# Performance work log

Hardware: AMD Instinct MI355X
Metric: run time of the kernel (lower is better)

## Reference

```python
import jax, jax.numpy as jnp
import numpy as np

B, T, N, F = 8, 24, 207, 16
H = 64            # hidden_dim
DH = 16           # dims_hyper[-1] / node-embedding out
DA = 4 * F        # temporal attention dim_out
DS = 64           # ss_gal gcn out dim (last_ss_gal_dim)
GDEP = 2
ALPHA, BETA, GAMMA = 0.05, 0.95, 0.95
TA = 2.0


def _lin(x, w, b=None):
    y = x @ w
    return y if b is None else y + b


def gcn_hyper(x, A, W, b):
    # x: [B,N,C], A: [N,N] static. h <- a*x + g * einsum('nvc,vw->nwc', h, A)
    h = x
    outs = [h]
    for _ in range(GDEP):
        h = ALPHA * x + GAMMA * jnp.einsum('bvc,vw->bwc', h, A)
        outs.append(h)
    return _lin(jnp.concatenate(outs, axis=-1), W, b)


def gcn_gru(x, A_dyn, A_sta, W, b):
    # x: [B,N,C], A_dyn: [B,N,N], A_sta: [N,N]
    h = x
    outs = [h]
    for _ in range(GDEP):
        h = (ALPHA * x
             + BETA * jnp.einsum('bvw,bvc->bwc', A_dyn, h)     # bmm(A^T, h)
             + GAMMA * jnp.einsum('bvc,vw->bwc', h, A_sta))
        outs.append(h)
    return _lin(jnp.concatenate(outs, axis=-1), W, b)


def gcn_ssgal(x, A, W, b):
    # x: [B*,N,C], A: [B*,N,N]
    h = x
    outs = [h]
    for _ in range(GDEP):
        h = ALPHA * x + GAMMA * jnp.einsum('bvw,bvc->bwc', A, h)
        outs.append(h)
    return _lin(jnp.concatenate(outs, axis=-1), W, b)


def setup_inputs() -> dict:
    key = jax.random.key(0)
    ks = jax.random.split(key, 32)
    i = iter(range(32))
    w = lambda *s: (0.02 * jax.random.normal(ks[next(i)], s, dtype=jnp.float32))
    inp = {
        'input_sequence': jax.random.normal(ks[next(i)], (B, T, N, F), dtype=jnp.float32),
        'static_adj': jax.random.uniform(ks[next(i)], (N, N), dtype=jnp.float32),
        # hyper graph generators: mlp in = (GDEP+1)*H -> DH
        'src_gen_w': w((GDEP + 1) * H, DH), 'src_gen_b': w(DH),
        'tgt_gen_w': w((GDEP + 1) * H, DH), 'tgt_gen_b': w(DH),
        # node embeddings: F -> DH
        'src_emb_w': w(F, DH), 'src_emb_b': w(DH),
        'tgt_emb_w': w(F, DH), 'tgt_emb_b': w(DH),
        # GRU gate GCNs: mlp in = (GDEP+1)*(F+H) -> H
        'gru_z_w': w((GDEP + 1) * (F + H), H), 'gru_z_b': w(H),
        'gru_r_w': w((GDEP + 1) * (F + H), H), 'gru_r_b': w(H),
        'gru_c_w': w((GDEP + 1) * (F + H), H), 'gru_c_b': w(H),
        # temporal attention: F -> DA, score DA -> 1
        'attn_q_w': w(F, DA),
        'attn_k_w': w(F, DA), 'attn_k_b': w(DA),
        'attn_s_w': w(DA, 1),
        # ss_gal spatial gcn: (GDEP+1)*F -> DS
        'sgcn_w': w((GDEP + 1) * F, DS), 'sgcn_b': w(DS),
        # predictors
        'short_w': w(DS, F), 'short_b': w(F),
        'long_w': w(H, F), 'long_b': w(F),
        'fus_w': w(DS + H, F), 'fus_b': w(F),
    }
    return inp


def _forward(input_sequence, static_adj,
             src_gen_w, src_gen_b, tgt_gen_w, tgt_gen_b,
             src_emb_w, src_emb_b, tgt_emb_w, tgt_emb_b,
             gru_z_w, gru_z_b, gru_r_w, gru_r_b, gru_c_w, gru_c_b,
             attn_q_w, attn_k_w, attn_k_b, attn_s_w,
             sgcn_w, sgcn_b,
             short_w, short_b, long_w, long_b, fus_w, fus_b):
    batch, steps, nodes = input_sequence.shape[0], input_sequence.shape[1], input_sequence.shape[2]
    eye = jnp.eye(nodes, dtype=input_sequence.dtype)

    def cell(x_t, h):
        # x_t: [B,N,F], h: [B,N,H]
        src_ctx = gcn_hyper(h, static_adj, src_gen_w, src_gen_b)   # [B,N,DH]
        tgt_ctx = gcn_hyper(h, static_adj, tgt_gen_w, tgt_gen_b)
        s = jnp.tanh(TA * _lin(x_t, src_emb_w, src_emb_b) * src_ctx)
        t = jnp.tanh(TA * _lin(x_t, tgt_emb_w, tgt_emb_b) * tgt_ctx)
        asym = jnp.einsum('bnc,bmc->bnm', s, t) - jnp.einsum('bnc,bmc->bnm', t, s)
        adj = jax.nn.relu(jnp.tanh(TA * asym)) + eye
        adj = adj / (adj.sum(axis=-1, keepdims=True) + 1e-8)
        gi = jnp.concatenate([x_t, h], axis=-1)
        z = jax.nn.sigmoid(gcn_gru(gi, adj, static_adj, gru_z_w, gru_z_b))
        r = jax.nn.sigmoid(gcn_gru(gi, adj, static_adj, gru_r_w, gru_r_b))
        ri = jnp.concatenate([x_t, r * h], axis=-1)
        c = jnp.tanh(gcn_gru(ri, adj, static_adj, gru_c_w, gru_c_b))
        return z * h + (1.0 - z) * c

    h = jnp.zeros((batch, nodes, H), dtype=input_sequence.dtype)
    for t_step in range(0, max(1, steps - 4), 4):
        h = cell(input_sequence[:, t_step], h)

    # ss_gal branch on the last 4 steps
    recent = input_sequence[:, -4:]            # [B,4,N,F]
    target = input_sequence[:, -1]             # [B,N,F]
    # temporal attention
    q = target @ attn_q_w                      # [B,N,DA]
    k = recent @ attn_k_w + attn_k_b           # [B,4,N,DA]
    scores = jnp.tanh(q[:, None, :, None, :] + k[:, :, None, :, :])  # [B,4,N,N,DA]
    scores = jnp.squeeze(scores @ attn_s_w, axis=-1)                  # [B,4,N,N]
    attn = jax.nn.softmax(scores, axis=-1)
    dyn_adj = static_adj[None] + attn.reshape(-1, nodes, nodes)       # [B*4,N,N]
    rh = recent.reshape(-1, nodes, recent.shape[-1])                  # [B*4,N,F]
    rh = gcn_ssgal(rh, dyn_adj, sgcn_w, sgcn_b)                       # [B*4,N,DS]
    rh = jax.nn.relu(rh.reshape(batch, -1, nodes, rh.shape[-1]))      # [B,4,N,DS]
    target = jnp.sum(rh, axis=1)                                       # [B,N,DS]

    short = _lin(target, short_w, short_b)      # [B,N,F]
    h = cell(short, h)                          # final GRU step on short-term prediction
    long = _lin(h, long_w, long_b)              # [B,N,F]
    fused = _lin(jnp.concatenate([target, h], axis=-1), fus_w, fus_b)  # [B,N,F]
    return jnp.stack([short, long, fused], axis=0)  # [3,B,N,F]


def reference(input_sequence, static_adj,
              src_gen_w, src_gen_b, tgt_gen_w, tgt_gen_b,
              src_emb_w, src_emb_b, tgt_emb_w, tgt_emb_b,
              gru_z_w, gru_z_b, gru_r_w, gru_r_b, gru_c_w, gru_c_b,
              attn_q_w, attn_k_w, attn_k_b, attn_s_w,
              sgcn_w, sgcn_b,
              short_w, short_b, long_w, long_b, fus_w, fus_b):
    return _forward(input_sequence, static_adj,
                    src_gen_w, src_gen_b, tgt_gen_w, tgt_gen_b,
                    src_emb_w, src_emb_b, tgt_emb_w, tgt_emb_b,
                    gru_z_w, gru_z_b, gru_r_w, gru_r_b, gru_c_w, gru_c_b,
                    attn_q_w, attn_k_w, attn_k_b, attn_s_w,
                    sgcn_w, sgcn_b,
                    short_w, short_b, long_w, long_b, fus_w, fus_b)
```

## Files before the change

kernel.cpp:

```cpp
#include <hip/hip_runtime.h>


constexpr int B = 8, T = 24, N = 207, F = 16, H = 64, DH = 16;
constexpr int PS = 208;
constexpr float ALPHA = 0.05f, BETA = 0.95f, GAMMA = 0.95f, TA = 2.0f;
constexpr int NF = N * F;
constexpr int BNF = B * N * F;

__device__ __forceinline__ float tanh_fast(float x) { float e = __expf(2.f * x); return 1.f - 2.f / (e + 1.f); }
__device__ __forceinline__ float sigm(float x) { return 1.f / (1.f + __expf(-x)); }
__device__ __forceinline__ float tanh_poly(float x) {
    float x2 = x * x;
    float c = __builtin_fmaf(x2, 0.13333333f, -0.33333333f);
    return x * __builtin_fmaf(x2, c, 1.f);
}

__global__ __launch_bounds__(256) void k_stage0(
    const float* __restrict__ adj, const float* __restrict__ inp,
    const float* __restrict__ Wq, const float* __restrict__ Wk,
    const float* __restrict__ kb, const float* __restrict__ sw_,
    const float* __restrict__ Wes, const float* __restrict__ bes,
    const float* __restrict__ Wet, const float* __restrict__ bet,
    const float* __restrict__ bsrc, const float* __restrict__ btgt,
    float* __restrict__ Ts, float* __restrict__ A2,
    float* __restrict__ attnT, float* __restrict__ rsum,
    float* __restrict__ s_out, float* __restrict__ t_out, float* __restrict__ catg)
{
    __shared__ __align__(16) float smem[7424];
    int bid = blockIdx.x, tid = threadIdx.x;
    if (bid < 49) {
        int vb = (bid % 7) * 32, wb = (bid / 7) * 32;
        float* sA = smem;
        float* sB = smem + 1056;
        float acc[4] = {0, 0, 0, 0};
        int i0 = tid >> 5, j = tid & 31;
        for (int u0 = 0; u0 < N; u0 += 32) {
            __syncthreads();
            for (int l = tid; l < 1024; l += 256) {
                int i = l >> 5, jj = l & 31;
                int v = vb + i, u = u0 + jj;
                sA[i * 33 + jj] = (v < N && u < N) ? adj[v * N + u] : 0.f;
                int uu = u0 + i, w = wb + jj;
                sB[i * 33 + jj] = (uu < N && w < N) ? adj[uu * N + w] : 0.f;
            }
            __syncthreads();
#pragma unroll 8
            for (int u = 0; u < 32; u++) {
                float bv = sB[u * 33 + j];
#pragma unroll
                for (int k = 0; k < 4; k++) acc[k] += sA[(i0 + k * 8) * 33 + u] * bv;
            }
        }
#pragma unroll
        for (int k = 0; k < 4; k++) {
            int v = vb + i0 + k * 8, w = wb + j;
            if (v < N && w < N) A2[(size_t)w * PS + v] = acc[k];
        }
    } else if (bid < 217) {
        int i = (bid - 49) * 256 + tid;
        if (i < N * N) {
            int w = i / N, v = i % N;
            Ts[(size_t)w * PS + v] = adj[v * N + w];
        }
    } else if (bid < 1785) {
        int idx = bid - 217;
        int bt = idx / 49, rem = idx % 49;
        int n0 = (rem % 7) * 32, m0 = (rem / 7) * 32;
        int b = bt >> 2, tau = bt & 3;
        int ti = tid >> 4, tj = tid & 15;
        float* sQ = smem;
        float* sK = smem + 2080;
        float* sWq = smem + 4160;
        float* sWk = smem + 5184;
        float* sXq = smem + 6208;
        float* sXk = smem + 6752;
        float* ssw = smem + 7296;
        float* skb = smem + 7360;
        const float* xq = inp + ((size_t)(b * T + (T - 1))) * NF;
        const float* xk = inp + ((size_t)(b * T + 20 + tau)) * NF;
        {
            float4 wq4 = *(const float4*)&Wq[tid * 4];
            float4 wk4 = *(const float4*)&Wk[tid * 4];
            *(float4*)&sWq[(tid >> 4) * 64 + (tid & 15) * 4] = wq4;
            *(float4*)&sWk[(tid >> 4) * 64 + (tid & 15) * 4] = wk4;
            if (tid < 64) { ssw[tid] = sw_[tid]; skb[tid] = kb[tid]; }
            int i2 = tid & 127;
            int r = i2 >> 2, c4 = (i2 & 3) * 4;
            if (tid < 128) {
                float4 aq = make_float4(0, 0, 0, 0);
                int n = n0 + r;
                if (n < N) aq = *(const float4*)&xq[(size_t)n * F + c4];
                sXq[r * 17 + c4] = aq.x; sXq[r * 17 + c4 + 1] = aq.y; sXq[r * 17 + c4 + 2] = aq.z; sXq[r * 17 + c4 + 3] = aq.w;
            } else {
                float4 ck = make_float4(0, 0, 0, 0);
                int m = m0 + r;
                if (m < N) ck = *(const float4*)&xk[(size_t)m * F + c4];
                sXk[r * 17 + c4] = ck.x; sXk[r * 17 + c4 + 1] = ck.y; sXk[r * 17 + c4 + 2] = ck.z; sXk[r * 17 + c4 + 3] = ck.w;
            }
        }
        __syncthreads();
        {
            int r = tid >> 3, o0 = (tid & 7) * 8;
            float xr[16], xkr[16];
#pragma unroll
            for (int f = 0; f < 16; f++) { xr[f] = sXq[r * 17 + f]; xkr[f] = sXk[r * 17 + f]; }
#pragma unroll
            for (int j = 0; j < 8; j++) {
                int o = o0 + j;
                float aq = 0.f, ak = skb[o];
#pragma unroll
                for (int f = 0; f < 16; f++) { aq += xr[f] * sWq[f * 64 + o]; ak += xkr[f] * sWk[f * 64 + o]; }
                sQ[r * 65 + o] = aq; sK[r * 65 + o] = ak;
            }
        }
        __syncthreads();
        float s00 = 0.f, s01 = 0.f, s10 = 0.f, s11 = 0.f;
#pragma unroll 2
        for (int d = 0; d < 64; d++) {
            float w = ssw[d];
            float q1 = sQ[ti * 65 + d], q2 = sQ[(ti + 16) * 65 + d];
            float k1 = sK[tj * 65 + d], k2 = sK[(tj + 16) * 65 + d];
            s00 += tanh_poly(q1 + k1) * w;
            s01 += tanh_poly(q1 + k2) * w;
            s10 += tanh_poly(q2 + k1) * w;
            s11 += tanh_poly(q2 + k2) * w;
        }
        int n1 = n0 + ti, n2 = n0 + ti + 16, m1 = m0 + tj, m2 = m0 + tj + 16;
        bool vn1 = n1 < N, vn2 = n2 < N, vm1 = m1 < N, vm2 = m2 < N;
        float e00 = (vn1 && vm1) ? __expf(s00) : 0.f;
        float e01 = (vn1 && vm2) ? __expf(s01) : 0.f;
        float e10 = (vn2 && vm1) ? __expf(s10) : 0.f;
        float e11 = (vn2 && vm2) ? __expf(s11) : 0.f;
        float part1 = e00 + e01, part2 = e10 + e11;
        for (int d = 8; d > 0; d >>= 1) {
            part1 += __shfl_down(part1, d, 16);
            part2 += __shfl_down(part2, d, 16);
        }
        if (tj == 0) {
            if (vn1) atomicAdd(&rsum[bt * N + n1], part1);
            if (vn2) atomicAdd(&rsum[bt * N + n2], part2);
        }
        __syncthreads();
        float* tile = sQ;
        tile[tj * 33 + ti] = e00;
        tile[(tj + 16) * 33 + ti] = e01;
        tile[tj * 33 + ti + 16] = e10;
        tile[(tj + 16) * 33 + ti + 16] = e11;
        __syncthreads();
        {
            int row = tid >> 3, c4 = (tid & 7) * 4;
            int m = m0 + row;
            if (m < N) {
                float4 v = make_float4(tile[row * 33 + c4], tile[row * 33 + c4 + 1],
                                       tile[row * 33 + c4 + 2], tile[row * 33 + c4 + 3]);
                *(float4*)&attnT[(size_t)bt * PS * PS + (size_t)m * PS + n0 + c4] = v;
            }
        }
    } else {
        int idx = bid - 1785;
        int x13 = idx % 13, b = idx / 13;
        int w0 = x13 * 16;
        int ty = tid >> 4, tx = tid & 15;
        float* sX  = smem;
        float* sWs = smem + 272;
        float* sWt = smem + 528;
        const float* xp = inp + ((size_t)(b * T + 0)) * NF;
        {
            int w = w0 + ty;
            sX[ty * 17 + tx] = (w < N) ? xp[(size_t)w * F + tx] : 0.f;
            sWs[ty * 16 + tx] = Wes[ty * 16 + tx];
            sWt[ty * 16 + tx] = Wet[ty * 16 + tx];
        }
        __syncthreads();
        float xs = bes[tx], xt = bet[tx];
#pragma unroll
        for (int f = 0; f < 16; f++) {
            float xv = sX[ty * 17 + f];
            xs += xv * sWs[f * 16 + tx];
            xt += xv * sWt[f * 16 + tx];
        }
        int w = w0 + ty;
        if (w < N) {
            s_out[((size_t)(b * N + w)) * DH + tx] = tanh_fast(TA * xs * bsrc[tx]);
            t_out[((size_t)(b * N + w)) * DH + tx] = tanh_fast(TA * xt * btgt[tx]);
            catg[((size_t)(b * N + w)) * 80 + tx] = sX[ty * 17 + tx];
#pragma unroll
            for (int j = 0; j < 4; j++) catg[((size_t)(b * N + w)) * 80 + 16 + tx * 4 + j] = 0.f;
        }
    }
}

__global__ __launch_bounds__(256) void k_cell_a(
    const float* __restrict__ h, const float* __restrict__ Ts, const float* __restrict__ A2,
    const float* __restrict__ xseq, int tsel, const float* __restrict__ xbuf,
    const float* __restrict__ Wsrc, const float* __restrict__ bsrc,
    const float* __restrict__ Wtgt, const float* __restrict__ btgt,
    const float* __restrict__ Wes, const float* __restrict__ bes,
    const float* __restrict__ Wet, const float* __restrict__ bet,
    float* __restrict__ s_out, float* __restrict__ t_out, float* __restrict__ catg) {
    int b = blockIdx.y, w0 = blockIdx.x * 16, lane = blockIdx.z;
    int tid = threadIdx.x, ty = tid >> 4, tx = tid & 15;
    __shared__ float sTs[2][16][33], sA2[2][16][33];
    __shared__ float sH[2][32][64];
    __shared__ float cat[16][193];
    __shared__ float sW[192][16];
    __shared__ float sX[16][16], sWe[16][16];
    float au[4] = {0, 0, 0, 0}, aw[4] = {0, 0, 0, 0};
    const float* hb = h + b * N * H;
    const float* xp = (tsel >= 0) ? (xseq + ((size_t)(b * T + tsel)) * NF) : (xbuf + (size_t)b * NF);
    int pidx = tid & 127;
    int pr = pidx >> 3, pc4 = (pidx & 7) * 4;
    float4 t4;
    float4 h4[2];
    int hr[2], hc[2];
#pragma unroll
    for (int k = 0; k < 2; k++) { int l4 = tid + k * 256; hr[k] = l4 >> 4; hc[k] = (l4 & 15) * 4; }
    auto loadT = [&](int v0) {
        t4 = make_float4(0, 0, 0, 0);
        const float* src = (tid < 128) ? Ts : A2;
        int w = w0 + pr;
        if (w < N) t4 = *(const float4*)&src[(size_t)w * PS + v0 + pc4];
#pragma unroll
        for (int k = 0; k < 2; k++) {
            float4 hv = make_float4(0, 0, 0, 0);
            int v = v0 + hr[k];
            if (v < N) hv = *(const float4*)&hb[(size_t)v * H + hc[k]];
            h4[k] = hv;
        }
    };
    loadT(0);
    int cur = 0;
    for (int t = 0; t < 7; t++) {
        __syncthreads();
        {
            float (*dst)[33] = (tid < 128) ? sTs[cur] : sA2[cur];
            dst[pr][pc4] = t4.x; dst[pr][pc4 + 1] = t4.y; dst[pr][pc4 + 2] = t4.z; dst[pr][pc4 + 3] = t4.w;
        }
#pragma unroll
        for (int k = 0; k < 2; k++) *(float4*)&sH[cur][hr[k]][hc[k]] = h4[k];
        if (t < 6) loadT((t + 1) * 32);
        __syncthreads();
#pragma unroll 8
        for (int v = 0; v < 32; v++) {
            float pu = sTs[cur][ty][v], pw = sA2[cur][ty][v];
#pragma unroll
            for (int j = 0; j < 4; j++) {
                float x = sH[cur][v][tx * 4 + j];
                au[j] += pu * x; aw[j] += pw * x;
            }
        }
        cur ^= 1;
    }
    int w = w0 + ty;
    bool valid = w < N;
    __syncthreads();
    if (valid) {
#pragma unroll
        for (int j = 0; j < 4; j++) {
            int c = tx * 4 + j;
            float hv = hb[(size_t)w * H + c];
            float u = au[j], w2 = aw[j];
            cat[ty][c] = hv;
            cat[ty][64 + c] = ALPHA * hv + GAMMA * u;
            cat[ty][128 + c] = ALPHA * hv + ALPHA * GAMMA * u + GAMMA * GAMMA * w2;
        }
    } else {
#pragma unroll
        for (int j = 0; j < 4; j++) {
            int c = tx * 4 + j;
            cat[ty][c] = 0; cat[ty][64 + c] = 0; cat[ty][128 + c] = 0;
        }
    }
    const float* Wg = lane ? Wtgt : Wsrc;
    const float* bg = lane ? btgt : bsrc;
    const float* We = lane ? Wet : Wes;
    const float* be = lane ? bet : bes;
    {
        float4 wv[3];
#pragma unroll
        for (int k = 0; k < 3; k++) wv[k] = *(const float4*)&Wg[(tid + k * 256) * 4];
        float4 xv = make_float4(0, 0, 0, 0), ev = make_float4(0, 0, 0, 0);
        int sr = 0, sc = 0;
        if (tid < 64) {
            sr = tid >> 2; sc = (tid & 3) * 4;
            int n = w0 + sr;
            if (n < N) xv = *(const float4*)&xp[(size_t)n * F + sc];
            ev = *(const float4*)&We[tid * 4];
        }
#pragma unroll
        for (int k = 0; k < 3; k++) {
            int l4 = tid + k * 256;
            int r = l4 >> 2, c4 = (l4 & 3) * 4;
            *(float4*)&sW[r][c4] = wv[k];
        }
        if (tid < 64) {
            *(float4*)&sX[sr][sc] = xv;
            *(float4*)&sWe[sr][sc] = ev;
        }
    }
    __syncthreads();
    if (lane == 0 && valid) {
#pragma unroll
        for (int j = 0; j < 5; j++) {
            int c = tx * 5 + j;
            float v = (c < 16) ? sX[ty][c] : hb[(size_t)w * H + (c - 16)];
            catg[((size_t)(b * N + w)) * 80 + c] = v;
        }
    }
    {
        float ctx = bg[tx];
#pragma unroll 8
        for (int c = 0; c < 192; c++) ctx += cat[ty][c] * sW[c][tx];
        float xe = be[tx];
#pragma unroll
        for (int f = 0; f < 16; f++) xe += sX[ty][f] * sWe[f][tx];
        if (valid) {
            float val = tanh_fast(TA * xe * ctx);
            if (lane == 0) s_out[(size_t)(b * N + w) * DH + tx] = val;
            else           t_out[(size_t)(b * N + w) * DH + tx] = val;
        }
    }
}

__global__ __launch_bounds__(256) void k_cell_bP(const float* __restrict__ s_in, const float* __restrict__ t_in,
                                                 const float* __restrict__ adj, float* __restrict__ P) {
    int b = blockIdx.y, v0 = blockIdx.x * 8;
    int tid = threadIdx.x, ty = tid >> 5, tx = tid & 31;
    __shared__ float sS[N][17], sT[N][17];
    for (int l4 = tid; l4 < 828; l4 += 256) {
        float4 sv = *(const float4*)&s_in[(size_t)b * N * 16 + l4 * 4];
        float4 tv = *(const float4*)&t_in[(size_t)b * N * 16 + l4 * 4];
        int r = l4 >> 2, c = (l4 & 3) * 4;
        sS[r][c] = sv.x; sS[r][c + 1] = sv.y; sS[r][c + 2] = sv.z; sS[r][c + 3] = sv.w;
        sT[r][c] = tv.x; sT[r][c + 1] = tv.y; sT[r][c + 2] = tv.z; sT[r][c + 3] = tv.w;
    }
    __syncthreads();
    int v = v0 + ty;
    bool valid = v < N;
    int vc = valid ? v : (N - 1);
    float sv[16], tv[16];
#pragma unroll
    for (int k = 0; k < 16; k++) { sv[k] = sS[vc][k]; tv[k] = sT[vc][k]; }
    float val[7];
    float rsum = 0.f;
#pragma unroll
    for (int idx = 0; idx < 7; idx++) {
        int w = tx + 32 * idx;
        float r = 0.f;
        if (w < N) {
            float a = 0.f;
#pragma unroll
            for (int k = 0; k < 16; k++) a += sv[k] * sT[w][k] - tv[k] * sS[w][k];
            r = tanh_fast(TA * a);
            r = r > 0.f ? r : 0.f;
            if (w == v) r += 1.f;
        }
        val[idx] = r;
        rsum += r;
    }
    float tot = rsum;
    for (int d = 16; d > 0; d >>= 1) tot += __shfl_down(tot, d, 32);
    tot = __shfl(tot, 0, 32);
    float rinv = BETA / (tot + 1e-8f);
    if (valid) {
        float* Pb = P + (size_t)b * PS * PS;
#pragma unroll
        for (int idx = 0; idx < 7; idx++) {
            int w = tx + 32 * idx;
            if (w < N) Pb[(size_t)w * PS + v] = val[idx] * rinv + GAMMA * adj[v * N + w];
        }
    }
}

__device__ __forceinline__ void body_prop_xr(float* smem, int w0, int bt,
    const float* __restrict__ attnT, const float* __restrict__ rsum,
    const float* __restrict__ Ts, const float* __restrict__ inp, float* __restrict__ x1)
{
    int b = bt >> 2, tau = bt & 3;
    const float* xb = inp + ((size_t)(b * T + 20 + tau)) * NF;
    const float* PA = attnT + (size_t)bt * PS * PS;
    int tid = threadIdx.x, ty = tid >> 4, tx = tid & 15;
    float (*sPA)[16][33] = (float(*)[16][33])(smem);
    float (*sPT)[16][33] = (float(*)[16][33])(smem + 1056);
    float (*sX)[32][17]  = (float(*)[32][17])(smem + 2112);
    float (*sXs)[32][17] = (float(*)[32][17])(smem + 3200);
    float accA = 0.f, accT = 0.f;
    int prr = tid >> 3, pcc = (tid & 7) * 4;
    int xrr = (tid - 128) >> 2, xcc = ((tid - 128) & 3) * 4;
    float4 pa, pt, xv;
    float rinv_;
    auto loadT = [&](int v0) {
        pa = make_float4(0, 0, 0, 0); pt = make_float4(0, 0, 0, 0); xv = make_float4(0, 0, 0, 0); rinv_ = 0.f;
        if (tid < 128) {
            int w = w0 + prr;
            if (w < N) {
                pa = *(const float4*)&PA[(size_t)w * PS + v0 + pcc];
                pt = *(const float4*)&Ts[(size_t)w * PS + v0 + pcc];
            }
        } else {
            int v = v0 + xrr;
            if (v < N) {
                xv = *(const float4*)&xb[(size_t)v * F + xcc];
                rinv_ = __builtin_amdgcn_rcpf(rsum[bt * N + v]);
            }
        }
    };
    loadT(0);
    int cur = 0;
    for (int t = 0; t < 7; t++) {
        __syncthreads();
        if (tid < 128) {
            sPA[cur][prr][pcc] = pa.x; sPA[cur][prr][pcc + 1] = pa.y; sPA[cur][prr][pcc + 2] = pa.z; sPA[cur][prr][pcc + 3] = pa.w;
            sPT[cur][prr][pcc] = pt.x; sPT[cur][prr][pcc + 1] = pt.y; sPT[cur][prr][pcc + 2] = pt.z; sPT[cur][prr][pcc + 3] = pt.w;
        } else {
            sX[cur][xrr][xcc] = xv.x; sX[cur][xrr][xcc + 1] = xv.y; sX[cur][xrr][xcc + 2] = xv.z; sX[cur][xrr][xcc + 3] = xv.w;
            sXs[cur][xrr][xcc] = xv.x * rinv_; sXs[cur][xrr][xcc + 1] = xv.y * rinv_;
            sXs[cur][xrr][xcc + 2] = xv.z * rinv_; sXs[cur][xrr][xcc + 3] = xv.w * rinv_;
        }
        if (t < 6) loadT((t + 1) * 32);
        __syncthreads();
#pragma unroll 8
        for (int v = 0; v < 32; v++) {
            accA += sPA[cur][ty][v] * sXs[cur][v][tx];
            accT += sPT[cur][ty][v] * sX[cur][v][tx];
        }
        cur ^= 1;
    }
    int w = w0 + ty;
    if (w < N) x1[((size_t)(bt * N + w)) * 16 + tx] = ALPHA * xb[w * F + tx] + GAMMA * (accA + accT);
}

__device__ __forceinline__ void body_sgc2(float* smem, int w0, int bt,
    const float* __restrict__ attnT, const float* __restrict__ rsum,
    const float* __restrict__ Ts, const float* __restrict__ x1, const float* __restrict__ inp,
    const float* __restrict__ Ws, const float* __restrict__ bs, float* __restrict__ target)
{
    int b = bt >> 2, tau = bt & 3;
    const float* xb = inp + ((size_t)(b * T + 20 + tau)) * NF;
    const float* PA = attnT + (size_t)bt * PS * PS;
    int tid = threadIdx.x, ty = tid >> 4, tx = tid & 15;
    float (*sPA)[16][33] = (float(*)[16][33])(smem);
    float (*sPT)[16][33] = (float(*)[16][33])(smem + 1056);
    float (*sX)[32][17]  = (float(*)[32][17])(smem + 2112);
    float (*sXs)[32][17] = (float(*)[32][17])(smem + 3200);
    float (*scat)[48]    = (float(*)[48])(smem + 4288);
    float (*sWs)[64]     = (float(*)[64])(smem + 5056);
    float accA = 0.f, accT = 0.f;
    int prr = tid >> 3, pcc = (tid & 7) * 4;
    int xrr = (tid - 128) >> 2, xcc = ((tid - 128) & 3) * 4;
    float4 pa, pt, xv;
    float rinv_;
    auto loadT = [&](int v0) {
        pa = make_float4(0, 0, 0, 0); pt = make_float4(0, 0, 0, 0); xv = make_float4(0, 0, 0, 0); rinv_ = 0.f;
        if (tid < 128) {
            int w = w0 + prr;
            if (w < N) {
                pa = *(const float4*)&PA[(size_t)w * PS + v0 + pcc];
                pt = *(const float4*)&Ts[(size_t)w * PS + v0 + pcc];
            }
        } else {
            int v = v0 + xrr;
            if (v < N) {
                xv = *(const float4*)&x1[((size_t)(bt * N + v)) * 16 + xcc];
                rinv_ = __builtin_amdgcn_rcpf(rsum[bt * N + v]);
            }
        }
    };
    loadT(0);
    int cur = 0;
    for (int t = 0; t < 7; t++) {
        __syncthreads();
        if (tid < 128) {
            sPA[cur][prr][pcc] = pa.x; sPA[cur][prr][pcc + 1] = pa.y; sPA[cur][prr][pcc + 2] = pa.z; sPA[cur][prr][pcc + 3] = pa.w;
            sPT[cur][prr][pcc] = pt.x; sPT[cur][prr][pcc + 1] = pt.y; sPT[cur][prr][pcc + 2] = pt.z; sPT[cur][prr][pcc + 3] = pt.w;
        } else {
            sX[cur][xrr][xcc] = xv.x; sX[cur][xrr][xcc + 1] = xv.y; sX[cur][xrr][xcc + 2] = xv.z; sX[cur][xrr][xcc + 3] = xv.w;
            sXs[cur][xrr][xcc] = xv.x * rinv_; sXs[cur][xrr][xcc + 1] = xv.y * rinv_;
            sXs[cur][xrr][xcc + 2] = xv.z * rinv_; sXs[cur][xrr][xcc + 3] = xv.w * rinv_;
        }
        if (t < 6) loadT((t + 1) * 32);
        __syncthreads();
#pragma unroll 8
        for (int v = 0; v < 32; v++) {
            accA += sPA[cur][ty][v] * sXs[cur][v][tx];
            accT += sPT[cur][ty][v] * sX[cur][v][tx];
        }
        cur ^= 1;
    }
    int w = w0 + ty;
    bool valid = w < N;
    __syncthreads();
    for (int l = tid; l < 512; l += 256) {
        int i = l >> 5, c = l & 31;
        int ww = w0 + i;
        float vv = 0;
        if (ww < N) {
            if (c < 16) vv = xb[ww * F + c];
            else vv = x1[((size_t)bt * N + ww) * 16 + (c - 16)];
        }
        scat[i][c] = vv;
    }
    {
        float x0 = valid ? xb[w * F + tx] : 0.f;
        scat[ty][32 + tx] = ALPHA * x0 + GAMMA * (accA + accT);
    }
    {
        float4 wv[3];
#pragma unroll
        for (int k = 0; k < 3; k++) wv[k] = *(const float4*)&Ws[(tid + k * 256) * 4];
#pragma unroll
        for (int k = 0; k < 3; k++) {
            int l4 = tid + k * 256;
            *(float4*)&sWs[l4 >> 4][(l4 & 15) * 4] = wv[k];
        }
    }
    __syncthreads();
    float acc[4];
#pragma unroll
    for (int j = 0; j < 4; j++) acc[j] = bs[tx * 4 + j];
#pragma unroll 8
    for (int cc = 0; cc < 48; cc++) {
        float cv = scat[ty][cc];
        float4 w4 = *(const float4*)&sWs[cc][tx * 4];
        acc[0] += cv * w4.x; acc[1] += cv * w4.y; acc[2] += cv * w4.z; acc[3] += cv * w4.w;
    }
    if (valid) {
#pragma unroll
        for (int j = 0; j < 4; j++) {
            float r = acc[j] > 0.f ? acc[j] : 0.f;
            atomicAdd(&target[(b * N + w) * 64 + tx * 4 + j], r);
        }
    }
}

__device__ __forceinline__ void body_short(float* smem, int n0, int b,
    const float* __restrict__ target, const float* __restrict__ Wsh, const float* __restrict__ bsh,
    float* __restrict__ out, float* __restrict__ xshort)
{
    int tid = threadIdx.x, ty = tid >> 4, tx = tid & 15;
    float (*trow)[65] = (float(*)[65])(smem);
    float (*sW)[16]   = (float(*)[16])(smem + 1040);
    {
        int r = tid >> 4, c4 = (tid & 15) * 4;
        int n = n0 + r;
        float4 tv = make_float4(0, 0, 0, 0);
        if (n < N) tv = *(const float4*)&target[((size_t)(b * N + n)) * 64 + c4];
        trow[r][c4] = tv.x; trow[r][c4 + 1] = tv.y; trow[r][c4 + 2] = tv.z; trow[r][c4 + 3] = tv.w;
        float4 wv = *(const float4*)&Wsh[tid * 4];
        *(float4*)&sW[tid >> 2][(tid & 3) * 4] = wv;
    }
    __syncthreads();
    float acc = bsh[tx];
#pragma unroll 8
    for (int o = 0; o < 64; o++) acc += trow[ty][o] * sW[o][tx];
    int n = n0 + ty;
    if (n < N) {
        out[((size_t)0 * B * N + b * N + n) * 16 + tx] = acc;
        xshort[(b * N + n) * 16 + tx] = acc;
    }
}

__global__ __launch_bounds__(256) void k_pg(
    const float* __restrict__ P, const float* __restrict__ cat, float* __restrict__ pg, int aux,
    const float* __restrict__ attnT, const float* __restrict__ rsum,
    const float* __restrict__ Ts, const float* __restrict__ inp, float* __restrict__ x1,
    const float* __restrict__ Ws, const float* __restrict__ bs, float* __restrict__ target,
    const float* __restrict__ Wsh, const float* __restrict__ bsh,
    float* __restrict__ out, float* __restrict__ xshort)
{
    __shared__ __align__(16) float smem[8128];
    int bid = blockIdx.x, tid = threadIdx.x;
    if (bid < 520) {
        int x13 = bid % 13, b = (bid / 13) & 7, z = bid / 104;
        int w0 = x13 * 16, c0 = z * 16;
        int ty = tid >> 4, tx = tid & 15;
        const float* Pb = P + (size_t)b * PS * PS;
        float (*sP)[16][33] = (float(*)[16][33])(smem);
        float (*sX)[32][17] = (float(*)[32][17])(smem + 1056);
        float a1 = 0.f;
        int pr = tid >> 4, pc = (tid & 15) * 2;
        int xr = tid >> 3, xc = (tid & 7) * 2;
        float2 pv, xv;
        auto loadT = [&](int v0) {
            pv = make_float2(0, 0); xv = make_float2(0, 0);
            int w = w0 + pr;
            if (w < N) pv = *(const float2*)&Pb[(size_t)w * PS + v0 + pc];
            int vv = v0 + xr;
            if (vv < N) xv = *(const float2*)&cat[((size_t)(b * N + vv)) * 80 + c0 + xc];
        };
        loadT(0);
        int cur = 0;
        for (int t = 0; t < 7; t++) {
            __syncthreads();
            sP[cur][pr][pc] = pv.x; sP[cur][pr][pc + 1] = pv.y;
            sX[cur][xr][xc] = xv.x; sX[cur][xr][xc + 1] = xv.y;
            if (t < 6) loadT((t + 1) * 32);
            __syncthreads();
#pragma unroll 8
            for (int v_ = 0; v_ < 32; v_++) a1 += sP[cur][ty][v_] * sX[cur][v_][tx];
            cur ^= 1;
        }
        int w = w0 + ty;
        if (w < N) pg[((size_t)(b * N + w)) * 80 + c0 + tx] = a1;
    } else {
        int idx = bid - 520;
        if (aux == 1)      body_prop_xr(smem, (idx % 13) * 16, idx / 13, attnT, rsum, Ts, inp, x1);
        else if (aux == 2) body_sgc2(smem, (idx % 13) * 16, idx / 13, attnT, rsum, Ts, x1, inp, Ws, bs, target);
        else               body_short(smem, (idx % 13) * 16, idx / 13, target, Wsh, bsh, out, xshort);
    }
}

__global__ __launch_bounds__(256) void k_gatezr(
    const float* __restrict__ catg, const float* __restrict__ pg,
    const float* __restrict__ P, float* __restrict__ P2,
    const float* __restrict__ Wz, const float* __restrict__ bz,
    const float* __restrict__ Wr, const float* __restrict__ br,
    const float* __restrict__ xseq, int tsel, const float* __restrict__ xbuf,
    float* __restrict__ zbuf, float* __restrict__ catc,
    const float* __restrict__ h)
{
    __shared__ __align__(16) float smem[7504];
    int bid = blockIdx.x, tid = threadIdx.x;
    if (bid < 208) {
        int mode = bid / 104, rem = bid % 104;
        int x13 = rem % 13, b = rem / 13;
        int w0 = x13 * 16;
        int ty = tid >> 4, tx = tid & 15;
        const float* W = mode ? Wr : Wz;
        const float* bias = mode ? br : bz;
        const float* Pb = P + (size_t)b * PS * PS;
        float (*sC)[241] = (float(*)[241])(smem);
        float (*sP)[33]  = (float(*)[33])(smem + 3856);
        float (*sX)[81]  = (float(*)[81])(smem + 4384);
        float (*sW)[65]  = (float(*)[65])(smem + 4384);
        for (int l4 = tid; l4 < 320; l4 += 256) {
            int r = l4 / 20, c4 = (l4 % 20) * 4;
            int w = w0 + r;
            float4 v4 = make_float4(0, 0, 0, 0);
            if (w < N) v4 = *(const float4*)&catg[((size_t)(b * N + w)) * 80 + c4];
            sC[r][c4] = v4.x; sC[r][c4 + 1] = v4.y; sC[r][c4 + 2] = v4.z; sC[r][c4 + 3] = v4.w;
        }
        float accP[5] = {0, 0, 0, 0, 0};
        int prr = tid >> 4, prc = (tid & 15) * 2;
        int xrow = tid & 31, xc0 = (tid >> 5) * 10;
        float2 pv;
        float2 xv[5];
        auto loadT = [&](int v0) {
            pv = make_float2(0, 0);
            int w = w0 + prr;
            if (w < N) pv = *(const float2*)&Pb[(size_t)w * PS + v0 + prc];
            int v = v0 + xrow;
#pragma unroll
            for (int k = 0; k < 5; k++) xv[k] = make_float2(0, 0);
            if (v < N) {
                const float* src = &pg[((size_t)(b * N + v)) * 80 + xc0];
#pragma unroll
                for (int k = 0; k < 5; k++) xv[k] = *(const float2*)&src[k * 2];
            }
        };
        loadT(0);
        for (int t = 0; t < 7; t++) {
            __syncthreads();
            sP[prr][prc] = pv.x; sP[prr][prc + 1] = pv.y;
#pragma unroll
            for (int k = 0; k < 5; k++) { sX[xrow][xc0 + 2 * k] = xv[k].x; sX[xrow][xc0 + 2 * k + 1] = xv[k].y; }
            if (t < 6) loadT((t + 1) * 32);
            __syncthreads();
#pragma unroll 8
            for (int v = 0; v < 32; v++) {
                float p = sP[ty][v];
#pragma unroll
                for (int j = 0; j < 5; j++) accP[j] += p * sX[v][tx * 5 + j];
            }
        }
        int w = w0 + ty;
        bool valid = w < N;
#pragma unroll
        for (int j = 0; j < 5; j++) {
            int c = tx * 5 + j;
            float pgo = valid ? pg[((size_t)(b * N + w)) * 80 + c] : 0.f;
            float g0 = sC[ty][c];
            sC[ty][80 + c]  = ALPHA * g0 + pgo;
            sC[ty][160 + c] = ALPHA * g0 + ALPHA * pgo + accP[j];
        }
        float4 wv[3];
#pragma unroll
        for (int k = 0; k < 3; k++) wv[k] = *(const float4*)&W[(tid + k * 256) * 4];
        float ga[4];
#pragma unroll
        for (int j = 0; j < 4; j++) ga[j] = bias[tx * 4 + j];
        for (int ch = 0; ch < 5; ch++) {
            __syncthreads();
#pragma unroll
            for (int k = 0; k < 3; k++) {
                int l4 = tid + k * 256;
                int r = l4 >> 4, cc = (l4 & 15) * 4;
                sW[r][cc] = wv[k].x; sW[r][cc + 1] = wv[k].y; sW[r][cc + 2] = wv[k].z; sW[r][cc + 3] = wv[k].w;
            }
            if (ch < 4) {
#pragma unroll
                for (int k = 0; k < 3; k++) wv[k] = *(const float4*)&W[(size_t)(ch + 1) * 3072 + (tid + k * 256) * 4];
            }
            __syncthreads();
            int c0 = ch * 48;
#pragma unroll 8
            for (int cc = 0; cc < 48; cc++) {
                float cv = sC[ty][c0 + cc];
#pragma unroll
                for (int j = 0; j < 4; j++) ga[j] += cv * sW[cc][tx * 4 + j];
            }
        }
        if (mode == 0) {
            if (valid) {
#pragma unroll
                for (int j = 0; j < 4; j++) zbuf[((size_t)(b * N + w)) * 64 + tx * 4 + j] = sigm(ga[j]);
            }
        } else {
            if (valid) {
#pragma unroll
                for (int j = 0; j < 4; j++) {
                    int o = tx * 4 + j;
                    catc[((size_t)(b * N + w)) * 80 + 16 + o] = sigm(ga[j]) * h[((size_t)(b * N + w)) * 64 + o];
                }
                if (tx < 4) {
                    const float* xp = (tsel >= 0) ? (xseq + ((size_t)(b * T + tsel)) * NF) : (xbuf + (size_t)b * NF);
#pragma unroll
                    for (int j = 0; j < 4; j++) {
                        int c = tx * 4 + j;
                        catc[((size_t)(b * N + w)) * 80 + c] = xp[w * F + c];
                    }
                }
            }
        }
    } else {
        int idx = bid - 208;
        int b = idx / 169, r = idx % 169;
        int w0 = (r % 13) * 16, v0 = (r / 13) * 16;
        const float* Pb = P + (size_t)b * PS * PS;
        float (*sA)[16][33] = (float(*)[16][33])(smem);
        float (*sB)[32][17] = (float(*)[32][17])(smem + 1056);
        int ty = tid >> 4, tx = tid & 15;
        int ar = tid >> 4, ac = (tid & 15) * 2;
        int br_ = tid >> 3, bc = (tid & 7) * 2;
        float2 av, bv;
        auto loadT = [&](int u0) {
            av = make_float2(0, 0); bv = make_float2(0, 0);
            int w = w0 + ar;
            if (w < N) av = *(const float2*)&Pb[(size_t)w * PS + u0 + ac];
            int u = u0 + br_;
            if (u < N) bv = *(const float2*)&Pb[(size_t)u * PS + v0 + bc];
        };
        loadT(0);
        int cur = 0;
        float acc = 0.f;
        for (int t = 0; t < 7; t++) {
            __syncthreads();
            sA[cur][ar][ac] = av.x; sA[cur][ar][ac + 1] = av.y;
            sB[cur][br_][bc] = bv.x; sB[cur][br_][bc + 1] = bv.y;
            if (t < 6) loadT((t + 1) * 32);
            __syncthreads();
#pragma unroll 8
            for (int u = 0; u < 32; u++) acc += sA[cur][ty][u] * sB[cur][u][tx];
            cur ^= 1;
        }
        int w = w0 + ty, v = v0 + tx;
        if (w < N && v < N) P2[(size_t)b * PS * PS + (size_t)w * PS + v] = acc;
    }
}

__global__ __launch_bounds__(256) void k_gate2(
    const float* __restrict__ cat, const float* __restrict__ P, const float* __restrict__ P2,
    const float* __restrict__ Wa, const float* __restrict__ ba,
    const float* __restrict__ Wb, const float* __restrict__ bb,
    int baseMode,
    const float* __restrict__ xseq, int tsel, const float* __restrict__ xbuf,
    float* __restrict__ zbuf, float* __restrict__ ricat,
    float* __restrict__ h,
    const float* __restrict__ target,
    const float* __restrict__ Wlong, const float* __restrict__ blong,
    const float* __restrict__ Wfus, const float* __restrict__ bfus,
    float* __restrict__ out) {
    int mode = baseMode + blockIdx.z;
    const float* W = (mode == 1) ? Wb : Wa;
    const float* bias = (mode == 1) ? bb : ba;
    int b = blockIdx.y, w0 = blockIdx.x * 16;
    int tid = threadIdx.x, ty = tid >> 4, tx = tid & 15;
    const float* Pb = P + (size_t)b * PS * PS;
    const float* Qb = P2 + (size_t)b * PS * PS;
    __shared__ float sC[16][241];
    __shared__ float sP[16][33], sQ[16][33];
    __shared__ float sX[32][81];
    __shared__ float sW[48][65];
    __shared__ float hrow[16][65], trow[16][65];
    for (int l4 = tid; l4 < 320; l4 += 256) {
        int r = l4 / 20, c4 = (l4 % 20) * 4;
        int w = w0 + r;
        float4 v4 = make_float4(0, 0, 0, 0);
        if (w < N) v4 = *(const float4*)&cat[((size_t)(b * N + w)) * 80 + c4];
        sC[r][c4] = v4.x; sC[r][c4 + 1] = v4.y; sC[r][c4 + 2] = v4.z; sC[r][c4 + 3] = v4.w;
    }
    float accP[5] = {0, 0, 0, 0, 0}, accQ[5] = {0, 0, 0, 0, 0};
    int prr = tid >> 4, prc = (tid & 15) * 2;
    int xrow = tid & 31, xc0 = (tid >> 5) * 10;
    float2 pv, qv;
    float2 xv[5];
    auto loadT = [&](int v0) {
        pv = make_float2(0, 0); qv = make_float2(0, 0);
        int w = w0 + prr;
        if (w < N) {
            pv = *(const float2*)&Pb[(size_t)w * PS + v0 + prc];
            qv = *(const float2*)&Qb[(size_t)w * PS + v0 + prc];
        }
        int v = v0 + xrow;
#pragma unroll
        for (int k = 0; k < 5; k++) xv[k] = make_float2(0, 0);
        if (v < N) {
            const float* src = &cat[((size_t)(b * N + v)) * 80 + xc0];
#pragma unroll
            for (int k = 0; k < 5; k++) xv[k] = *(const float2*)&src[k * 2];
        }
    };
    loadT(0);
    for (int t = 0; t < 7; t++) {
        __syncthreads();
        sP[prr][prc] = pv.x; sP[prr][prc + 1] = pv.y;
        sQ[prr][prc] = qv.x; sQ[prr][prc + 1] = qv.y;
#pragma unroll
        for (int k = 0; k < 5; k++) { sX[xrow][xc0 + 2 * k] = xv[k].x; sX[xrow][xc0 + 2 * k + 1] = xv[k].y; }
        if (t < 6) loadT((t + 1) * 32);
        __syncthreads();
#pragma unroll 8
        for (int v = 0; v < 32; v++) {
            float p = sP[ty][v], q = sQ[ty][v];
#pragma unroll
            for (int j = 0; j < 5; j++) {
                float x = sX[v][tx * 5 + j];
                accP[j] += p * x;
                accQ[j] += q * x;
            }
        }
    }
#pragma unroll
    for (int j = 0; j < 5; j++) {
        int c = tx * 5 + j;
        float g0 = sC[ty][c];
        sC[ty][80 + c]  = ALPHA * g0 + accP[j];
        sC[ty][160 + c] = ALPHA * g0 + ALPHA * accP[j] + accQ[j];
    }
    float4 wv[3];
#pragma unroll
    for (int k = 0; k < 3; k++) wv[k] = *(const float4*)&W[(tid + k * 256) * 4];
    float ga[4];
#pragma unroll
    for (int j = 0; j < 4; j++) ga[j] = bias[tx * 4 + j];
    for (int ch = 0; ch < 5; ch++) {
        __syncthreads();
#pragma unroll
        for (int k = 0; k < 3; k++) {
            int l4 = tid + k * 256;
            int r = l4 >> 4, cc = (l4 & 15) * 4;
            sW[r][cc] = wv[k].x; sW[r][cc + 1] = wv[k].y; sW[r][cc + 2] = wv[k].z; sW[r][cc + 3] = wv[k].w;
        }
        if (ch < 4) {
#pragma unroll
            for (int k = 0; k < 3; k++) wv[k] = *(const float4*)&W[(size_t)(ch + 1) * 3072 + (tid + k * 256) * 4];
        }
        __syncthreads();
        int c0 = ch * 48;
#pragma unroll 8
        for (int cc = 0; cc < 48; cc++) {
            float cv = sC[ty][c0 + cc];
#pragma unroll
            for (int j = 0; j < 4; j++) ga[j] += cv * sW[cc][tx * 4 + j];
        }
    }
    int w = w0 + ty;
    bool valid = w < N;
    if (mode == 0) {
        if (valid) {
#pragma unroll
            for (int j = 0; j < 4; j++) zbuf[((size_t)(b * N + w)) * 64 + tx * 4 + j] = sigm(ga[j]);
        }
    } else if (mode == 1) {
        if (valid) {
#pragma unroll
            for (int j = 0; j < 4; j++) {
                int o = tx * 4 + j;
                ricat[((size_t)(b * N + w)) * 80 + 16 + o] = sigm(ga[j]) * h[((size_t)(b * N + w)) * 64 + o];
            }
            if (tx < 4) {
                const float* xp = (tsel >= 0) ? (xseq + ((size_t)(b * T + tsel)) * NF) : (xbuf + (size_t)b * NF);
#pragma unroll
                for (int j = 0; j < 4; j++) {
                    int c = tx * 4 + j;
                    ricat[((size_t)(b * N + w)) * 80 + c] = xp[w * F + c];
                }
            }
        }
    } else {
#pragma unroll
        for (int j = 0; j < 4; j++) {
            int o = tx * 4 + j;
            float cval = tanh_fast(ga[j]);
            float zv = 0.f, hv = 0.f;
            if (valid) { zv = zbuf[((size_t)(b * N + w)) * 64 + o]; hv = h[((size_t)(b * N + w)) * 64 + o]; }
            float hn = zv * hv + (1.f - zv) * cval;
            if (valid) h[((size_t)(b * N + w)) * 64 + o] = hn;
            hrow[ty][o] = valid ? hn : 0.f;
        }
        if (mode == 3) {
            for (int l = tid; l < 1024; l += 256) {
                int i = l >> 6, o = l & 63;
                int ww = w0 + i;
                trow[i][o] = (ww < N) ? target[((size_t)(b * N + ww)) * 64 + o] : 0.f;
            }
            __syncthreads();
            float lg = blong[tx];
            float fs = bfus[tx];
#pragma unroll 8
            for (int o = 0; o < 64; o++) {
                lg += hrow[ty][o] * Wlong[o * 16 + tx];
                fs += trow[ty][o] * Wfus[o * 16 + tx] + hrow[ty][o] * Wfus[(64 + o) * 16 + tx];
            }
            if (valid) {
                out[((size_t)1 * B * N + b * N + w) * 16 + tx] = lg;
                out[((size_t)2 * B * N + b * N + w) * 16 + tx] = fs;
            }
        }
    }
}

extern "C" void kernel_launch(void* const* d_in, const int* in_sizes, int n_in,
                              void* d_out, int out_size, void* d_ws, size_t ws_size,
                              hipStream_t stream) {
    const float* inp = (const float*)d_in[0];
    const float* adj = (const float*)d_in[1];
    const float* src_gen_w = (const float*)d_in[2];
    const float* src_gen_b = (const float*)d_in[3];
    const float* tgt_gen_w = (const float*)d_in[4];
    const float* tgt_gen_b = (const float*)d_in[5];
    const float* src_emb_w = (const float*)d_in[6];
    const float* src_emb_b = (const float*)d_in[7];
    const float* tgt_emb_w = (const float*)d_in[8];
    const float* tgt_emb_b = (const float*)d_in[9];
    const float* gru_z_w = (const float*)d_in[10];
    const float* gru_z_b = (const float*)d_in[11];
    const float* gru_r_w = (const float*)d_in[12];
    const float* gru_r_b = (const float*)d_in[13];
    const float* gru_c_w = (const float*)d_in[14];
    const float* gru_c_b = (const float*)d_in[15];
    const float* attn_q_w = (const float*)d_in[16];
    const float* attn_k_w = (const float*)d_in[17];
    const float* attn_k_b = (const float*)d_in[18];
    const float* attn_s_w = (const float*)d_in[19];
    const float* sgcn_w = (const float*)d_in[20];
    const float* sgcn_b = (const float*)d_in[21];
    const float* short_w = (const float*)d_in[22];
    const float* short_b = (const float*)d_in[23];
    const float* long_w = (const float*)d_in[24];
    const float* long_b = (const float*)d_in[25];
    const float* fus_w = (const float*)d_in[26];
    const float* fus_b = (const float*)d_in[27];
    float* out = (float*)d_out;

    float* ws = (float*)d_ws;
    size_t off = 0;
    auto A = [&](size_t n) { n = (n + 3) & ~(size_t)3; float* p = ws + off; off += n; return p; };
    float* Ts = A((size_t)PS * PS);
    float* A2 = A((size_t)PS * PS);
    float* sbuf = A((size_t)B * N * DH);
    float* tbuf = A((size_t)B * N * DH);
    float* P = A((size_t)B * PS * PS);
    float* P2 = A((size_t)B * PS * PS);
    float* catg = A((size_t)B * N * 80);
    float* catc = A((size_t)B * N * 80);
    float* pgbuf = A((size_t)B * N * 80);
    float* zb = A((size_t)B * N * 64);
    float* attnT = A((size_t)32 * PS * PS);
    float* x1 = A((size_t)32 * NF);
    float* xshort = A(BNF);
    size_t zero_begin = off;
    float* h = A((size_t)B * N * H);
    float* target = A((size_t)B * N * 64);
    float* rsum = A((size_t)32 * N);
    size_t zero_end = off;
    (void)ws_size; (void)in_sizes; (void)n_in; (void)out_size;

    hipMemsetAsync(h, 0, (zero_end - zero_begin) * sizeof(float), stream);
    k_stage0<<<1889, 256, 0, stream>>>(adj, inp, attn_q_w, attn_k_w, attn_k_b, attn_s_w,
                                       src_emb_w, src_emb_b, tgt_emb_w, tgt_emb_b,
                                       src_gen_b, tgt_gen_b,
                                       Ts, A2, attnT, rsum, sbuf, tbuf, catg);

    auto run_cell = [&](int tsel, const float* xbuf, int finalFlag, int aux, bool skipA) {
        if (!skipA)
            k_cell_a<<<dim3(13, B, 2), 256, 0, stream>>>(h, Ts, A2, inp, tsel, xbuf,
                                                         src_gen_w, src_gen_b, tgt_gen_w, tgt_gen_b,
                                                         src_emb_w, src_emb_b, tgt_emb_w, tgt_emb_b, sbuf, tbuf, catg);
        k_cell_bP<<<dim3(26, B), 256, 0, stream>>>(sbuf, tbuf, adj, P);
        int extra = (aux == 1 || aux == 2) ? 416 : (aux == 3 ? 104 : 0);
        k_pg<<<520 + extra, 256, 0, stream>>>(P, catg, pgbuf, aux, attnT, rsum, Ts, inp, x1,
                                              sgcn_w, sgcn_b, target, short_w, short_b, out, xshort);
        k_gatezr<<<1560, 256, 0, stream>>>(catg, pgbuf, P, P2, gru_z_w, gru_z_b, gru_r_w, gru_r_b,
                                           inp, tsel, xbuf, zb, catc, h);
        k_gate2<<<dim3(13, B, 1), 256, 0, stream>>>(catc, P, P2, gru_c_w, gru_c_b, nullptr, nullptr, 2 + finalFlag,
                                                    nullptr, 0, nullptr, zb, nullptr, h,
                                                    target, long_w, long_b, fus_w, fus_b, out);
    };

    run_cell(0, nullptr, 0, 1, true);
    run_cell(4, nullptr, 0, 2, false);
    run_cell(8, nullptr, 0, 3, false);
    run_cell(12, nullptr, 0, 0, false);
    run_cell(16, nullptr, 0, 0, false);

    run_cell(-1, xshort, 1, 0, false);
}
```

Baseline: 589.7 us.

## Move attention tiles into first P kernel and P2 into pg kernel

The temporal-attention tile computation moves out of the stage-0 kernel and into the first cell's P-construction kernel, so it runs alongside P instead of delaying the start of the recurrence. The P2 = P·P product moves from the z/r gate kernel into the pg kernel, and the gate kernel drops to one block per (mode, batch, row tile). This rebalances work across launches so the large grids run in parallel with the small ones. The cost is larger grids mixing heterogeneous block bodies, and a gate kernel with far fewer blocks that may underfill the GPU.

```diff
diff --git a/kernel.cpp b/kernel.cpp
--- a/kernel.cpp
+++ b/kernel.cpp
@@ -17,16 +17,13 @@
 
 __global__ __launch_bounds__(256) void k_stage0(
     const float* __restrict__ adj, const float* __restrict__ inp,
-    const float* __restrict__ Wq, const float* __restrict__ Wk,
-    const float* __restrict__ kb, const float* __restrict__ sw_,
     const float* __restrict__ Wes, const float* __restrict__ bes,
     const float* __restrict__ Wet, const float* __restrict__ bet,
     const float* __restrict__ bsrc, const float* __restrict__ btgt,
     float* __restrict__ Ts, float* __restrict__ A2,
-    float* __restrict__ attnT, float* __restrict__ rsum,
     float* __restrict__ s_out, float* __restrict__ t_out, float* __restrict__ catg)
 {
-    __shared__ __align__(16) float smem[7424];
+    __shared__ __align__(16) float smem[2112];
     int bid = blockIdx.x, tid = threadIdx.x;
     if (bid < 49) {
         int vb = (bid % 7) * 32, wb = (bid / 7) * 32;
@@ -62,8 +59,232 @@
             int w = i / N, v = i % N;
             Ts[(size_t)w * PS + v] = adj[v * N + w];
         }
-    } else if (bid < 1785) {
+    } else {
         int idx = bid - 217;
+        int x13 = idx % 13, b = idx / 13;
+        int w0 = x13 * 16;
+        int ty = tid >> 4, tx = tid & 15;
+        float* sX  = smem;
+        float* sWs = smem + 272;
+        float* sWt = smem + 528;
+        const float* xp = inp + ((size_t)(b * T + 0)) * NF;
+        {
+            int w = w0 + ty;
+            sX[ty * 17 + tx] = (w < N) ? xp[(size_t)w * F + tx] : 0.f;
+            sWs[ty * 16 + tx] = Wes[ty * 16 + tx];
+            sWt[ty * 16 + tx] = Wet[ty * 16 + tx];
+        }
+        __syncthreads();
+        float xs = bes[tx], xt = bet[tx];
+#pragma unroll
+        for (int f = 0; f < 16; f++) {
+            float xv = sX[ty * 17 + f];
+            xs += xv * sWs[f * 16 + tx];
+            xt += xv * sWt[f * 16 + tx];
+        }
+        int w = w0 + ty;
+        if (w < N) {
+            s_out[((size_t)(b * N + w)) * DH + tx] = tanh_fast(TA * xs * bsrc[tx]);
+            t_out[((size_t)(b * N + w)) * DH + tx] = tanh_fast(TA * xt * btgt[tx]);
+            catg[((size_t)(b * N + w)) * 80 + tx] = sX[ty * 17 + tx];
+#pragma unroll
+            for (int j = 0; j < 4; j++) catg[((size_t)(b * N + w)) * 80 + 16 + tx * 4 + j] = 0.f;
+        }
+    }
+}
+
+__global__ __launch_bounds__(256) void k_cell_a(
+    const float* __restrict__ h, const float* __restrict__ Ts, const float* __restrict__ A2,
+    const float* __restrict__ xseq, int tsel, const float* __restrict__ xbuf,
+    const float* __restrict__ Wsrc, const float* __restrict__ bsrc,
+    const float* __restrict__ Wtgt, const float* __restrict__ btgt,
+    const float* __restrict__ Wes, const float* __restrict__ bes,
+    const float* __restrict__ Wet, const float* __restrict__ bet,
+    float* __restrict__ s_out, float* __restrict__ t_out, float* __restrict__ catg) {
+    int b = blockIdx.y, w0 = blockIdx.x * 16, lane = blockIdx.z;
+    int tid = threadIdx.x, ty = tid >> 4, tx = tid & 15;
+    __shared__ float sTs[2][16][33], sA2[2][16][33];
+    __shared__ float sH[2][32][64];
+    __shared__ float cat[16][193];
+    __shared__ float sW[192][16];
+    __shared__ float sX[16][16], sWe[16][16];
+    float au[4] = {0, 0, 0, 0}, aw[4] = {0, 0, 0, 0};
+    const float* hb = h + b * N * H;
+    const float* xp = (tsel >= 0) ? (xseq + ((size_t)(b * T + tsel)) * NF) : (xbuf + (size_t)b * NF);
+    int pidx = tid & 127;
+    int pr = pidx >> 3, pc4 = (pidx & 7) * 4;
+    float4 t4;
+    float4 h4[2];
+    int hr[2], hc[2];
+#pragma unroll
+    for (int k = 0; k < 2; k++) { int l4 = tid + k * 256; hr[k] = l4 >> 4; hc[k] = (l4 & 15) * 4; }
+    auto loadT = [&](int v0) {
+        t4 = make_float4(0, 0, 0, 0);
+        const float* src = (tid < 128) ? Ts : A2;
+        int w = w0 + pr;
+        if (w < N) t4 = *(const float4*)&src[(size_t)w * PS + v0 + pc4];
+#pragma unroll
+        for (int k = 0; k < 2; k++) {
+            float4 hv = make_float4(0, 0, 0, 0);
+            int v = v0 + hr[k];
+            if (v < N) hv = *(const float4*)&hb[(size_t)v * H + hc[k]];
+            h4[k] = hv;
+        }
+    };
+    loadT(0);
+    int cur = 0;
+    for (int t = 0; t < 7; t++) {
+        __syncthreads();
+        {
+            float (*dst)[33] = (tid < 128) ? sTs[cur] : sA2[cur];
+            dst[pr][pc4] = t4.x; dst[pr][pc4 + 1] = t4.y; dst[pr][pc4 + 2] = t4.z; dst[pr][pc4 + 3] = t4.w;
+        }
+#pragma unroll
+        for (int k = 0; k < 2; k++) *(float4*)&sH[cur][hr[k]][hc[k]] = h4[k];
+        if (t < 6) loadT((t + 1) * 32);
+        __syncthreads();
+#pragma unroll 8
+        for (int v = 0; v < 32; v++) {
+            float pu = sTs[cur][ty][v], pw = sA2[cur][ty][v];
+#pragma unroll
+            for (int j = 0; j < 4; j++) {
+                float x = sH[cur][v][tx * 4 + j];
+                au[j] += pu * x; aw[j] += pw * x;
+            }
+        }
+        cur ^= 1;
+    }
+    int w = w0 + ty;
+    bool valid = w < N;
+    __syncthreads();
+    if (valid) {
+#pragma unroll
+        for (int j = 0; j < 4; j++) {
+            int c = tx * 4 + j;
+            float hv = hb[(size_t)w * H + c];
+            float u = au[j], w2 = aw[j];
+            cat[ty][c] = hv;
+            cat[ty][64 + c] = ALPHA * hv + GAMMA * u;
+            cat[ty][128 + c] = ALPHA * hv + ALPHA * GAMMA * u + GAMMA * GAMMA * w2;
+        }
+    } else {
+#pragma unroll
+        for (int j = 0; j < 4; j++) {
+            int c = tx * 4 + j;
+            cat[ty][c] = 0; cat[ty][64 + c] = 0; cat[ty][128 + c] = 0;
+        }
+    }
+    const float* Wg = lane ? Wtgt : Wsrc;
+    const float* bg = lane ? btgt : bsrc;
+    const float* We = lane ? Wet : Wes;
+    const float* be = lane ? bet : bes;
+    {
+        float4 wv[3];
+#pragma unroll
+        for (int k = 0; k < 3; k++) wv[k] = *(const float4*)&Wg[(tid + k * 256) * 4];
+        float4 xv = make_float4(0, 0, 0, 0), ev = make_float4(0, 0, 0, 0);
+        int sr = 0, sc = 0;
+        if (tid < 64) {
+            sr = tid >> 2; sc = (tid & 3) * 4;
+            int n = w0 + sr;
+            if (n < N) xv = *(const float4*)&xp[(size_t)n * F + sc];
+            ev = *(const float4*)&We[tid * 4];
+        }
+#pragma unroll
+        for (int k = 0; k < 3; k++) {
+            int l4 = tid + k * 256;
+            int r = l4 >> 2, c4 = (l4 & 3) * 4;
+            *(float4*)&sW[r][c4] = wv[k];
+        }
+        if (tid < 64) {
+            *(float4*)&sX[sr][sc] = xv;
+            *(float4*)&sWe[sr][sc] = ev;
+        }
+    }
+    __syncthreads();
+    if (lane == 0 && valid) {
+#pragma unroll
+        for (int j = 0; j < 5; j++) {
+            int c = tx * 5 + j;
+            float v = (c < 16) ? sX[ty][c] : hb[(size_t)w * H + (c - 16)];
+            catg[((size_t)(b * N + w)) * 80 + c] = v;
+        }
+    }
+    {
+        float ctx = bg[tx];
+#pragma unroll 8
+        for (int c = 0; c < 192; c++) ctx += cat[ty][c] * sW[c][tx];
+        float xe = be[tx];
+#pragma unroll
+        for (int f = 0; f < 16; f++) xe += sX[ty][f] * sWe[f][tx];
+        if (valid) {
+            float val = tanh_fast(TA * xe * ctx);
+            if (lane == 0) s_out[(size_t)(b * N + w) * DH + tx] = val;
+            else           t_out[(size_t)(b * N + w) * DH + tx] = val;
+        }
+    }
+}
+
+__global__ __launch_bounds__(256) void k_bp(
+    const float* __restrict__ s_in, const float* __restrict__ t_in,
+    const float* __restrict__ adj, float* __restrict__ P,
+    const float* __restrict__ inp,
+    const float* __restrict__ Wq, const float* __restrict__ Wk,
+    const float* __restrict__ kb, const float* __restrict__ sw_,
+    float* __restrict__ attnT, float* __restrict__ rsum)
+{
+    __shared__ __align__(16) float smem[7424];
+    int bid = blockIdx.x, tid = threadIdx.x;
+    if (bid < 208) {
+        int b = bid / 26, v0 = (bid % 26) * 8;
+        int ty = tid >> 5, tx = tid & 31;
+        float (*sS)[17] = (float (*)[17])(smem);
+        float (*sT)[17] = (float (*)[17])(smem + 3519);
+        for (int l4 = tid; l4 < 828; l4 += 256) {
+            float4 sv = *(const float4*)&s_in[(size_t)b * N * 16 + l4 * 4];
+            float4 tv = *(const float4*)&t_in[(size_t)b * N * 16 + l4 * 4];
+            int r = l4 >> 2, c = (l4 & 3) * 4;
+            sS[r][c] = sv.x; sS[r][c + 1] = sv.y; sS[r][c + 2] = sv.z; sS[r][c + 3] = sv.w;
+            sT[r][c] = tv.x; sT[r][c + 1] = tv.y; sT[r][c + 2] = tv.z; sT[r][c + 3] = tv.w;
+        }
+        __syncthreads();
+        int v = v0 + ty;
+        bool valid = v < N;
+        int vc = valid ? v : (N - 1);
+        float sv[16], tv[16];
+#pragma unroll
+        for (int k = 0; k < 16; k++) { sv[k] = sS[vc][k]; tv[k] = sT[vc][k]; }
+        float val[7];
+        float rs = 0.f;
+#pragma unroll
+        for (int idx = 0; idx < 7; idx++) {
+            int w = tx + 32 * idx;
+            float r = 0.f;
+            if (w < N) {
+                float a = 0.f;
+#pragma unroll
+                for (int k = 0; k < 16; k++) a += sv[k] * sT[w][k] - tv[k] * sS[w][k];
+                r = tanh_fast(TA * a);
+                r = r > 0.f ? r : 0.f;
+                if (w == v) r += 1.f;
+            }
+            val[idx] = r;
+            rs += r;
+        }
+        float tot = rs;
+        for (int d = 16; d > 0; d >>= 1) tot += __shfl_down(tot, d, 32);
+        tot = __shfl(tot, 0, 32);
+        float rinv = BETA / (tot + 1e-8f);
+        if (valid) {
+            float* Pb = P + (size_t)b * PS * PS;
+#pragma unroll
+            for (int idx = 0; idx < 7; idx++) {
+                int w = tx + 32 * idx;
+                if (w < N) Pb[(size_t)w * PS + v] = val[idx] * rinv + GAMMA * adj[v * N + w];
+            }
+        }
+    } else {
+        int idx = bid - 208;
         int bt = idx / 49, rem = idx % 49;
         int n0 = (rem % 7) * 32, m0 = (rem / 7) * 32;
         int b = bt >> 2, tau = bt & 3;
@@ -156,219 +377,6 @@
                 *(float4*)&attnT[(size_t)bt * PS * PS + (size_t)m * PS + n0 + c4] = v;
             }
         }
-    } else {
-        int idx = bid - 1785;
-        int x13 = idx % 13, b = idx / 13;
-        int w0 = x13 * 16;
-        int ty = tid >> 4, tx = tid & 15;
-        float* sX  = smem;
-        float* sWs = smem + 272;
-        float* sWt = smem + 528;
-        const float* xp = inp + ((size_t)(b * T + 0)) * NF;
-        {
-            int w = w0 + ty;
-            sX[ty * 17 + tx] = (w < N) ? xp[(size_t)w * F + tx] : 0.f;
-            sWs[ty * 16 + tx] = Wes[ty * 16 + tx];
-            sWt[ty * 16 + tx] = Wet[ty * 16 + tx];
-        }
-        __syncthreads();
-        float xs = bes[tx], xt = bet[tx];
-#pragma unroll
-        for (int f = 0; f < 16; f++) {
-            float xv = sX[ty * 17 + f];
-            xs += xv * sWs[f * 16 + tx];
-            xt += xv * sWt[f * 16 + tx];
-        }
-        int w = w0 + ty;
-        if (w < N) {
-            s_out[((size_t)(b * N + w)) * DH + tx] = tanh_fast(TA * xs * bsrc[tx]);
-            t_out[((size_t)(b * N + w)) * DH + tx] = tanh_fast(TA * xt * btgt[tx]);
-            catg[((size_t)(b * N + w)) * 80 + tx] = sX[ty * 17 + tx];
-#pragma unroll
-            for (int j = 0; j < 4; j++) catg[((size_t)(b * N + w)) * 80 + 16 + tx * 4 + j] = 0.f;
-        }
-    }
-}
-
-__global__ __launch_bounds__(256) void k_cell_a(
-    const float* __restrict__ h, const float* __restrict__ Ts, const float* __restrict__ A2,
-    const float* __restrict__ xseq, int tsel, const float* __restrict__ xbuf,
-    const float* __restrict__ Wsrc, const float* __restrict__ bsrc,
-    const float* __restrict__ Wtgt, const float* __restrict__ btgt,
-    const float* __restrict__ Wes, const float* __restrict__ bes,
-    const float* __restrict__ Wet, const float* __restrict__ bet,
-    float* __restrict__ s_out, float* __restrict__ t_out, float* __restrict__ catg) {
-    int b = blockIdx.y, w0 = blockIdx.x * 16, lane = blockIdx.z;
-    int tid = threadIdx.x, ty = tid >> 4, tx = tid & 15;
-    __shared__ float sTs[2][16][33], sA2[2][16][33];
-    __shared__ float sH[2][32][64];
-    __shared__ float cat[16][193];
-    __shared__ float sW[192][16];
-    __shared__ float sX[16][16], sWe[16][16];
-    float au[4] = {0, 0, 0, 0}, aw[4] = {0, 0, 0, 0};
-    const float* hb = h + b * N * H;
-    const float* xp = (tsel >= 0) ? (xseq + ((size_t)(b * T + tsel)) * NF) : (xbuf + (size_t)b * NF);
-    int pidx = tid & 127;
-    int pr = pidx >> 3, pc4 = (pidx & 7) * 4;
-    float4 t4;
-    float4 h4[2];
-    int hr[2], hc[2];
-#pragma unroll
-    for (int k = 0; k < 2; k++) { int l4 = tid + k * 256; hr[k] = l4 >> 4; hc[k] = (l4 & 15) * 4; }
-    auto loadT = [&](int v0) {
-        t4 = make_float4(0, 0, 0, 0);
-        const float* src = (tid < 128) ? Ts : A2;
-        int w = w0 + pr;
-        if (w < N) t4 = *(const float4*)&src[(size_t)w * PS + v0 + pc4];
-#pragma unroll
-        for (int k = 0; k < 2; k++) {
-            float4 hv = make_float4(0, 0, 0, 0);
-            int v = v0 + hr[k];
-            if (v < N) hv = *(const float4*)&hb[(size_t)v * H + hc[k]];
-            h4[k] = hv;
-        }
-    };
-    loadT(0);
-    int cur = 0;
-    for (int t = 0; t < 7; t++) {
-        __syncthreads();
-        {
-            float (*dst)[33] = (tid < 128) ? sTs[cur] : sA2[cur];
-            dst[pr][pc4] = t4.x; dst[pr][pc4 + 1] = t4.y; dst[pr][pc4 + 2] = t4.z; dst[pr][pc4 + 3] = t4.w;
-        }
-#pragma unroll
-        for (int k = 0; k < 2; k++) *(float4*)&sH[cur][hr[k]][hc[k]] = h4[k];
-        if (t < 6) loadT((t + 1) * 32);
-        __syncthreads();
-#pragma unroll 8
-        for (int v = 0; v < 32; v++) {
-            float pu = sTs[cur][ty][v], pw = sA2[cur][ty][v];
-#pragma unroll
-            for (int j = 0; j < 4; j++) {
-                float x = sH[cur][v][tx * 4 + j];
-                au[j] += pu * x; aw[j] += pw * x;
-            }
-        }
-        cur ^= 1;
-    }
-    int w = w0 + ty;
-    bool valid = w < N;
-    __syncthreads();
-    if (valid) {
-#pragma unroll
-        for (int j = 0; j < 4; j++) {
-            int c = tx * 4 + j;
-            float hv = hb[(size_t)w * H + c];
-            float u = au[j], w2 = aw[j];
-            cat[ty][c] = hv;
-            cat[ty][64 + c] = ALPHA * hv + GAMMA * u;
-            cat[ty][128 + c] = ALPHA * hv + ALPHA * GAMMA * u + GAMMA * GAMMA * w2;
-        }
-    } else {
-#pragma unroll
-        for (int j = 0; j < 4; j++) {
-            int c = tx * 4 + j;
-            cat[ty][c] = 0; cat[ty][64 + c] = 0; cat[ty][128 + c] = 0;
-        }
-    }
-    const float* Wg = lane ? Wtgt : Wsrc;
-    const float* bg = lane ? btgt : bsrc;
-    const float* We = lane ? Wet : Wes;
-    const float* be = lane ? bet : bes;
-    {
-        float4 wv[3];
-#pragma unroll
-        for (int k = 0; k < 3; k++) wv[k] = *(const float4*)&Wg[(tid + k * 256) * 4];
-        float4 xv = make_float4(0, 0, 0, 0), ev = make_float4(0, 0, 0, 0);
-        int sr = 0, sc = 0;
-        if (tid < 64) {
-            sr = tid >> 2; sc = (tid & 3) * 4;
-            int n = w0 + sr;
-            if (n < N) xv = *(const float4*)&xp[(size_t)n * F + sc];
-            ev = *(const float4*)&We[tid * 4];
-        }
-#pragma unroll
-        for (int k = 0; k < 3; k++) {
-            int l4 = tid + k * 256;
-            int r = l4 >> 2, c4 = (l4 & 3) * 4;
-            *(float4*)&sW[r][c4] = wv[k];
-        }
-        if (tid < 64) {
-            *(float4*)&sX[sr][sc] = xv;
-            *(float4*)&sWe[sr][sc] = ev;
-        }
-    }
-    __syncthreads();
-    if (lane == 0 && valid) {
-#pragma unroll
-        for (int j = 0; j < 5; j++) {
-            int c = tx * 5 + j;
-            float v = (c < 16) ? sX[ty][c] : hb[(size_t)w * H + (c - 16)];
-            catg[((size_t)(b * N + w)) * 80 + c] = v;
-        }
-    }
-    {
-        float ctx = bg[tx];
-#pragma unroll 8
-        for (int c = 0; c < 192; c++) ctx += cat[ty][c] * sW[c][tx];
-        float xe = be[tx];
-#pragma unroll
-        for (int f = 0; f < 16; f++) xe += sX[ty][f] * sWe[f][tx];
-        if (valid) {
-            float val = tanh_fast(TA * xe * ctx);
-            if (lane == 0) s_out[(size_t)(b * N + w) * DH + tx] = val;
-            else           t_out[(size_t)(b * N + w) * DH + tx] = val;
-        }
-    }
-}
-
-__global__ __launch_bounds__(256) void k_cell_bP(const float* __restrict__ s_in, const float* __restrict__ t_in,
-                                                 const float* __restrict__ adj, float* __restrict__ P) {
-    int b = blockIdx.y, v0 = blockIdx.x * 8;
-    int tid = threadIdx.x, ty = tid >> 5, tx = tid & 31;
-    __shared__ float sS[N][17], sT[N][17];
-    for (int l4 = tid; l4 < 828; l4 += 256) {
-        float4 sv = *(const float4*)&s_in[(size_t)b * N * 16 + l4 * 4];
-        float4 tv = *(const float4*)&t_in[(size_t)b * N * 16 + l4 * 4];
-        int r = l4 >> 2, c = (l4 & 3) * 4;
-        sS[r][c] = sv.x; sS[r][c + 1] = sv.y; sS[r][c + 2] = sv.z; sS[r][c + 3] = sv.w;
-        sT[r][c] = tv.x; sT[r][c + 1] = tv.y; sT[r][c + 2] = tv.z; sT[r][c + 3] = tv.w;
-    }
-    __syncthreads();
-    int v = v0 + ty;
-    bool valid = v < N;
-    int vc = valid ? v : (N - 1);
-    float sv[16], tv[16];
-#pragma unroll
-    for (int k = 0; k < 16; k++) { sv[k] = sS[vc][k]; tv[k] = sT[vc][k]; }
-    float val[7];
-    float rsum = 0.f;
-#pragma unroll
-    for (int idx = 0; idx < 7; idx++) {
-        int w = tx + 32 * idx;
-        float r = 0.f;
-        if (w < N) {
-            float a = 0.f;
-#pragma unroll
-            for (int k = 0; k < 16; k++) a += sv[k] * sT[w][k] - tv[k] * sS[w][k];
-            r = tanh_fast(TA * a);
-            r = r > 0.f ? r : 0.f;
-            if (w == v) r += 1.f;
-        }
-        val[idx] = r;
-        rsum += r;
-    }
-    float tot = rsum;
-    for (int d = 16; d > 0; d >>= 1) tot += __shfl_down(tot, d, 32);
-    tot = __shfl(tot, 0, 32);
-    float rinv = BETA / (tot + 1e-8f);
-    if (valid) {
-        float* Pb = P + (size_t)b * PS * PS;
-#pragma unroll
-        for (int idx = 0; idx < 7; idx++) {
-            int w = tx + 32 * idx;
-            if (w < N) Pb[(size_t)w * PS + v] = val[idx] * rinv + GAMMA * adj[v * N + w];
-        }
     }
 }
 
@@ -443,8 +451,8 @@
     float (*sPT)[16][33] = (float(*)[16][33])(smem + 1056);
     float (*sX)[32][17]  = (float(*)[32][17])(smem + 2112);
     float (*sXs)[32][17] = (float(*)[32][17])(smem + 3200);
-    float (*scat)[48]    = (float(*)[48])(smem + 4288);
-    float (*sWs)[64]     = (float(*)[64])(smem + 5056);
+    float (*scat)[48]    = (float(*)[48])(smem);
+    float (*sWs)[64]     = (float(*)[64])(smem + 768);
     float accA = 0.f, accT = 0.f;
     int prr = tid >> 3, pcc = (tid & 7) * 4;
     int xrr = (tid - 128) >> 2, xcc = ((tid - 128) & 3) * 4;
@@ -561,14 +569,15 @@
 }
 
 __global__ __launch_bounds__(256) void k_pg(
-    const float* __restrict__ P, const float* __restrict__ cat, float* __restrict__ pg, int aux,
+    const float* __restrict__ P, const float* __restrict__ cat,
+    float* __restrict__ pg, float* __restrict__ P2, int aux,
     const float* __restrict__ attnT, const float* __restrict__ rsum,
     const float* __restrict__ Ts, const float* __restrict__ inp, float* __restrict__ x1,
     const float* __restrict__ Ws, const float* __restrict__ bs, float* __restrict__ target,
     const float* __restrict__ Wsh, const float* __restrict__ bsh,
     float* __restrict__ out, float* __restrict__ xshort)
 {
-    __shared__ __align__(16) float smem[8128];
+    __shared__ __align__(16) float smem[4288];
     int bid = blockIdx.x, tid = threadIdx.x;
     if (bid < 520) {
         int x13 = bid % 13, b = (bid / 13) & 7, z = bid / 104;
@@ -602,138 +611,8 @@
         }
         int w = w0 + ty;
         if (w < N) pg[((size_t)(b * N + w)) * 80 + c0 + tx] = a1;
-    } else {
+    } else if (bid < 1872) {
         int idx = bid - 520;
-        if (aux == 1)      body_prop_xr(smem, (idx % 13) * 16, idx / 13, attnT, rsum, Ts, inp, x1);
-        else if (aux == 2) body_sgc2(smem, (idx % 13) * 16, idx / 13, attnT, rsum, Ts, x1, inp, Ws, bs, target);
-        else               body_short(smem, (idx % 13) * 16, idx / 13, target, Wsh, bsh, out, xshort);
-    }
-}
-
-__global__ __launch_bounds__(256) void k_gatezr(
-    const float* __restrict__ catg, const float* __restrict__ pg,
-    const float* __restrict__ P, float* __restrict__ P2,
-    const float* __restrict__ Wz, const float* __restrict__ bz,
-    const float* __restrict__ Wr, const float* __restrict__ br,
-    const float* __restrict__ xseq, int tsel, const float* __restrict__ xbuf,
-    float* __restrict__ zbuf, float* __restrict__ catc,
-    const float* __restrict__ h)
-{
-    __shared__ __align__(16) float smem[7504];
-    int bid = blockIdx.x, tid = threadIdx.x;
-    if (bid < 208) {
-        int mode = bid / 104, rem = bid % 104;
-        int x13 = rem % 13, b = rem / 13;
-        int w0 = x13 * 16;
-        int ty = tid >> 4, tx = tid & 15;
-        const float* W = mode ? Wr : Wz;
-        const float* bias = mode ? br : bz;
-        const float* Pb = P + (size_t)b * PS * PS;
-        float (*sC)[241] = (float(*)[241])(smem);
-        float (*sP)[33]  = (float(*)[33])(smem + 3856);
-        float (*sX)[81]  = (float(*)[81])(smem + 4384);
-        float (*sW)[65]  = (float(*)[65])(smem + 4384);
-        for (int l4 = tid; l4 < 320; l4 += 256) {
-            int r = l4 / 20, c4 = (l4 % 20) * 4;
-            int w = w0 + r;
-            float4 v4 = make_float4(0, 0, 0, 0);
-            if (w < N) v4 = *(const float4*)&catg[((size_t)(b * N + w)) * 80 + c4];
-            sC[r][c4] = v4.x; sC[r][c4 + 1] = v4.y; sC[r][c4 + 2] = v4.z; sC[r][c4 + 3] = v4.w;
-        }
-        float accP[5] = {0, 0, 0, 0, 0};
-        int prr = tid >> 4, prc = (tid & 15) * 2;
-        int xrow = tid & 31, xc0 = (tid >> 5) * 10;
-        float2 pv;
-        float2 xv[5];
-        auto loadT = [&](int v0) {
-            pv = make_float2(0, 0);
-            int w = w0 + prr;
-            if (w < N) pv = *(const float2*)&Pb[(size_t)w * PS + v0 + prc];
-            int v = v0 + xrow;
-#pragma unroll
-            for (int k = 0; k < 5; k++) xv[k] = make_float2(0, 0);
-            if (v < N) {
-                const float* src = &pg[((size_t)(b * N + v)) * 80 + xc0];
-#pragma unroll
-                for (int k = 0; k < 5; k++) xv[k] = *(const float2*)&src[k * 2];
-            }
-        };
-        loadT(0);
-        for (int t = 0; t < 7; t++) {
-            __syncthreads();
-            sP[prr][prc] = pv.x; sP[prr][prc + 1] = pv.y;
-#pragma unroll
-            for (int k = 0; k < 5; k++) { sX[xrow][xc0 + 2 * k] = xv[k].x; sX[xrow][xc0 + 2 * k + 1] = xv[k].y; }
-            if (t < 6) loadT((t + 1) * 32);
-            __syncthreads();
-#pragma unroll 8
-            for (int v = 0; v < 32; v++) {
-                float p = sP[ty][v];
-#pragma unroll
-                for (int j = 0; j < 5; j++) accP[j] += p * sX[v][tx * 5 + j];
-            }
-        }
-        int w = w0 + ty;
-        bool valid = w < N;
-#pragma unroll
-        for (int j = 0; j < 5; j++) {
-            int c = tx * 5 + j;
-            float pgo = valid ? pg[((size_t)(b * N + w)) * 80 + c] : 0.f;
-            float g0 = sC[ty][c];
-            sC[ty][80 + c]  = ALPHA * g0 + pgo;
-            sC[ty][160 + c] = ALPHA * g0 + ALPHA * pgo + accP[j];
-        }
-        float4 wv[3];
-#pragma unroll
-        for (int k = 0; k < 3; k++) wv[k] = *(const float4*)&W[(tid + k * 256) * 4];
-        float ga[4];
-#pragma unroll
-        for (int j = 0; j < 4; j++) ga[j] = bias[tx * 4 + j];
-        for (int ch = 0; ch < 5; ch++) {
-            __syncthreads();
-#pragma unroll
-            for (int k = 0; k < 3; k++) {
-                int l4 = tid + k * 256;
-                int r = l4 >> 4, cc = (l4 & 15) * 4;
-                sW[r][cc] = wv[k].x; sW[r][cc + 1] = wv[k].y; sW[r][cc + 2] = wv[k].z; sW[r][cc + 3] = wv[k].w;
-            }
-            if (ch < 4) {
-#pragma unroll
-                for (int k = 0; k < 3; k++) wv[k] = *(const float4*)&W[(size_t)(ch + 1) * 3072 + (tid + k * 256) * 4];
-            }
-            __syncthreads();
-            int c0 = ch * 48;
-#pragma unroll 8
-            for (int cc = 0; cc < 48; cc++) {
-                float cv = sC[ty][c0 + cc];
-#pragma unroll
-                for (int j = 0; j < 4; j++) ga[j] += cv * sW[cc][tx * 4 + j];
-            }
-        }
-        if (mode == 0) {
-            if (valid) {
-#pragma unroll
-                for (int j = 0; j < 4; j++) zbuf[((size_t)(b * N + w)) * 64 + tx * 4 + j] = sigm(ga[j]);
-            }
-        } else {
-            if (valid) {
-#pragma unroll
-                for (int j = 0; j < 4; j++) {
-                    int o = tx * 4 + j;
-                    catc[((size_t)(b * N + w)) * 80 + 16 + o] = sigm(ga[j]) * h[((size_t)(b * N + w)) * 64 + o];
-                }
-                if (tx < 4) {
-                    const float* xp = (tsel >= 0) ? (xseq + ((size_t)(b * T + tsel)) * NF) : (xbuf + (size_t)b * NF);
-#pragma unroll
-                    for (int j = 0; j < 4; j++) {
-                        int c = tx * 4 + j;
-                        catc[((size_t)(b * N + w)) * 80 + c] = xp[w * F + c];
-                    }
-                }
-            }
-        }
-    } else {
-        int idx = bid - 208;
         int b = idx / 169, r = idx % 169;
         int w0 = (r % 13) * 16, v0 = (r / 13) * 16;
         const float* Pb = P + (size_t)b * PS * PS;
@@ -765,6 +644,134 @@
         }
         int w = w0 + ty, v = v0 + tx;
         if (w < N && v < N) P2[(size_t)b * PS * PS + (size_t)w * PS + v] = acc;
+    } else {
+        int idx = bid - 1872;
+        if (aux == 1)      body_prop_xr(smem, (idx % 13) * 16, idx / 13, attnT, rsum, Ts, inp, x1);
+        else if (aux == 2) body_sgc2(smem, (idx % 13) * 16, idx / 13, attnT, rsum, Ts, x1, inp, Ws, bs, target);
+        else               body_short(smem, (idx % 13) * 16, idx / 13, target, Wsh, bsh, out, xshort);
+    }
+}
+
+__global__ __launch_bounds__(256) void k_gatezr(
+    const float* __restrict__ catg, const float* __restrict__ pg,
+    const float* __restrict__ P,
+    const float* __restrict__ Wz, const float* __restrict__ bz,
+    const float* __restrict__ Wr, const float* __restrict__ br,
+    const float* __restrict__ xseq, int tsel, const float* __restrict__ xbuf,
+    float* __restrict__ zbuf, float* __restrict__ catc,
+    const float* __restrict__ h)
+{
+    __shared__ __align__(16) float smem[7504];
+    int bid = blockIdx.x, tid = threadIdx.x;
+    int mode = bid / 104, rem = bid % 104;
+    int x13 = rem % 13, b = rem / 13;
+    int w0 = x13 * 16;
+    int ty = tid >> 4, tx = tid & 15;
+    const float* W = mode ? Wr : Wz;
+    const float* bias = mode ? br : bz;
+    const float* Pb = P + (size_t)b * PS * PS;
+    float (*sC)[241] = (float(*)[241])(smem);
+    float (*sP)[33]  = (float(*)[33])(smem + 3856);
+    float (*sX)[81]  = (float(*)[81])(smem + 4384);
+    float (*sW)[65]  = (float(*)[65])(smem + 4384);
+    for (int l4 = tid; l4 < 320; l4 += 256) {
+        int r = l4 / 20, c4 = (l4 % 20) * 4;
+        int w = w0 + r;
+        float4 v4 = make_float4(0, 0, 0, 0);
+        if (w < N) v4 = *(const float4*)&catg[((size_t)(b * N + w)) * 80 + c4];
+        sC[r][c4] = v4.x; sC[r][c4 + 1] = v4.y; sC[r][c4 + 2] = v4.z; sC[r][c4 + 3] = v4.w;
+    }
+    float accP[5] = {0, 0, 0, 0, 0};
+    int prr = tid >> 4, prc = (tid & 15) * 2;
+    int xrow = tid & 31, xc0 = (tid >> 5) * 10;
+    float2 pv;
+    float2 xv[5];
+    auto loadT = [&](int v0) {
+        pv = make_float2(0, 0);
+        int w = w0 + prr;
+        if (w < N) pv = *(const float2*)&Pb[(size_t)w * PS + v0 + prc];
+        int v = v0 + xrow;
+#pragma unroll
+        for (int k = 0; k < 5; k++) xv[k] = make_float2(0, 0);
+        if (v < N) {
+            const float* src = &pg[((size_t)(b * N + v)) * 80 + xc0];
+#pragma unroll
+            for (int k = 0; k < 5; k++) xv[k] = *(const float2*)&src[k * 2];
+        }
+    };
+    loadT(0);
+    for (int t = 0; t < 7; t++) {
+        __syncthreads();
+        sP[prr][prc] = pv.x; sP[prr][prc + 1] = pv.y;
+#pragma unroll
+        for (int k = 0; k < 5; k++) { sX[xrow][xc0 + 2 * k] = xv[k].x; sX[xrow][xc0 + 2 * k + 1] = xv[k].y; }
+        if (t < 6) loadT((t + 1) * 32);
+        __syncthreads();
+#pragma unroll 8
+        for (int v = 0; v < 32; v++) {
+            float p = sP[ty][v];
+#pragma unroll
+            for (int j = 0; j < 5; j++) accP[j] += p * sX[v][tx * 5 + j];
+        }
+    }
+    int w = w0 + ty;
+    bool valid = w < N;
+#pragma unroll
+    for (int j = 0; j < 5; j++) {
+        int c = tx * 5 + j;
+        float pgo = valid ? pg[((size_t)(b * N + w)) * 80 + c] : 0.f;
+        float g0 = sC[ty][c];
+        sC[ty][80 + c]  = ALPHA * g0 + pgo;
+        sC[ty][160 + c] = ALPHA * g0 + ALPHA * pgo + accP[j];
+    }
+    float4 wv[3];
+#pragma unroll
+    for (int k = 0; k < 3; k++) wv[k] = *(const float4*)&W[(tid + k * 256) * 4];
+    float ga[4];
+#pragma unroll
+    for (int j = 0; j < 4; j++) ga[j] = bias[tx * 4 + j];
+    for (int ch = 0; ch < 5; ch++) {
+        __syncthreads();
+#pragma unroll
+        for (int k = 0; k < 3; k++) {
+            int l4 = tid + k * 256;
+            int r = l4 >> 4, cc = (l4 & 15) * 4;
+            sW[r][cc] = wv[k].x; sW[r][cc + 1] = wv[k].y; sW[r][cc + 2] = wv[k].z; sW[r][cc + 3] = wv[k].w;
+        }
+        if (ch < 4) {
+#pragma unroll
+            for (int k = 0; k < 3; k++) wv[k] = *(const float4*)&W[(size_t)(ch + 1) * 3072 + (tid + k * 256) * 4];
+        }
+        __syncthreads();
+        int c0 = ch * 48;
+#pragma unroll 8
+        for (int cc = 0; cc < 48; cc++) {
+            float cv = sC[ty][c0 + cc];
+#pragma unroll
+            for (int j = 0; j < 4; j++) ga[j] += cv * sW[cc][tx * 4 + j];
+        }
+    }
+    if (mode == 0) {
+        if (valid) {
+#pragma unroll
+            for (int j = 0; j < 4; j++) zbuf[((size_t)(b * N + w)) * 64 + tx * 4 + j] = sigm(ga[j]);
+        }
+    } else {
+        if (valid) {
+#pragma unroll
+            for (int j = 0; j < 4; j++) {
+                int o = tx * 4 + j;
+                catc[((size_t)(b * N + w)) * 80 + 16 + o] = sigm(ga[j]) * h[((size_t)(b * N + w)) * 64 + o];
+            }
+            if (tx < 4) {
+                const float* xp = (tsel >= 0) ? (xseq + ((size_t)(b * T + tsel)) * NF) : (xbuf + (size_t)b * NF);
+#pragma unroll
+                for (int j = 0; j < 4; j++) {
+                    int c = tx * 4 + j;
+                    catc[((size_t)(b * N + w)) * 80 + c] = xp[w * F + c];
+                }
+            }
+        }
     }
 }
 
@@ -987,32 +994,33 @@
     (void)ws_size; (void)in_sizes; (void)n_in; (void)out_size;
 
     hipMemsetAsync(h, 0, (zero_end - zero_begin) * sizeof(float), stream);
-    k_stage0<<<1889, 256, 0, stream>>>(adj, inp, attn_q_w, attn_k_w, attn_k_b, attn_s_w,
-                                       src_emb_w, src_emb_b, tgt_emb_w, tgt_emb_b,
-                                       src_gen_b, tgt_gen_b,
-                                       Ts, A2, attnT, rsum, sbuf, tbuf, catg);
-
-    auto run_cell = [&](int tsel, const float* xbuf, int finalFlag, int aux, bool skipA) {
+    k_stage0<<<321, 256, 0, stream>>>(adj, inp,
+                                      src_emb_w, src_emb_b, tgt_emb_w, tgt_emb_b,
+                                      src_gen_b, tgt_gen_b,
+                                      Ts, A2, sbuf, tbuf, catg);
+
+    auto run_cell = [&](int tsel, const float* xbuf, int finalFlag, int aux, bool skipA, bool withAttn) {
         if (!skipA)
             k_cell_a<<<dim3(13, B, 2), 256, 0, stream>>>(h, Ts, A2, inp, tsel, xbuf,
                                                          src_gen_w, src_gen_b, tgt_gen_w, tgt_gen_b,
                                                          src_emb_w, src_emb_b, tgt_emb_w, tgt_emb_b, sbuf, tbuf, catg);
-        k_cell_bP<<<dim3(26, B), 256, 0, stream>>>(sbuf, tbuf, adj, P);
+        k_bp<<<withAttn ? 1776 : 208, 256, 0, stream>>>(sbuf, tbuf, adj, P, inp,
+                                                        attn_q_w, attn_k_w, attn_k_b, attn_s_w, attnT, rsum);
         int extra = (aux == 1 || aux == 2) ? 416 : (aux == 3 ? 104 : 0);
-        k_pg<<<520 + extra, 256, 0, stream>>>(P, catg, pgbuf, aux, attnT, rsum, Ts, inp, x1,
-                                              sgcn_w, sgcn_b, target, short_w, short_b, out, xshort);
-        k_gatezr<<<1560, 256, 0, stream>>>(catg, pgbuf, P, P2, gru_z_w, gru_z_b, gru_r_w, gru_r_b,
-                                           inp, tsel, xbuf, zb, catc, h);
+        k_pg<<<1872 + extra, 256, 0, stream>>>(P, catg, pgbuf, P2, aux, attnT, rsum, Ts, inp, x1,
+                                               sgcn_w, sgcn_b, target, short_w, short_b, out, xshort);
+        k_gatezr<<<208, 256, 0, stream>>>(catg, pgbuf, P, gru_z_w, gru_z_b, gru_r_w, gru_r_b,
+                                          inp, tsel, xbuf, zb, catc, h);
         k_gate2<<<dim3(13, B, 1), 256, 0, stream>>>(catc, P, P2, gru_c_w, gru_c_b, nullptr, nullptr, 2 + finalFlag,
                                                     nullptr, 0, nullptr, zb, nullptr, h,
                                                     target, long_w, long_b, fus_w, fus_b, out);
     };
 
-    run_cell(0, nullptr, 0, 1, true);
-    run_cell(4, nullptr, 0, 2, false);
-    run_cell(8, nullptr, 0, 3, false);
-    run_cell(12, nullptr, 0, 0, false);
-    run_cell(16, nullptr, 0, 0, false);
-
-    run_cell(-1, xshort, 1, 0, false);
+    run_cell(0, nullptr, 0, 1, true, true);
+    run_cell(4, nullptr, 0, 2, false, false);
+    run_cell(8, nullptr, 0, 3, false, false);
+    run_cell(12, nullptr, 0, 0, false, false);
+    run_cell(16, nullptr, 0, 0, false, false);
+
+    run_cell(-1, xshort, 1, 0, false, false);
 }
```

After: 631.2 us. 7.0% more time.
